# Kernel optimization log

Hardware: AMD Instinct MI355X
Metric: run time of the kernel (lower is better)

Reference implementation:

```python
import jax, jax.numpy as jnp
import numpy as np

B, C, H, W = 4, 64, 256, 256
HEADS = 4
HID = 128  # dim * ffn_expansion_factor
EPS = 1e-5


def _ln_chan(x, w, b):
    # LayerNorm over channel axis of [b,c,h,w] (equiv to to_3d -> LN over c -> to_4d)
    mu = x.mean(1, keepdims=True)
    var = jnp.mean((x - mu) ** 2, axis=1, keepdims=True)
    return (x - mu) / jnp.sqrt(var + EPS) * w[None, :, None, None] + b[None, :, None, None]


def _ln_last(x, w, b):
    mu = x.mean(-1, keepdims=True)
    var = jnp.mean((x - mu) ** 2, axis=-1, keepdims=True)
    return (x - mu) / jnp.sqrt(var + EPS) * w + b


def _conv1(x, Wt):
    # 1x1 conv, no bias; Wt: [out,in]
    return jnp.einsum('oi,bihw->bohw', Wt, x)


def _l2norm(x):
    # torch F.normalize(dim=-1): x / max(||x||, 1e-12)
    return x / jnp.maximum(jnp.linalg.norm(x, axis=-1, keepdims=True), 1e-12)


def _dct(inp1, inp2, Wq, Wk, Wv, temp):
    # Divide_Cross_Transformer: q from inp2, k/v from inp1; channel-wise attention
    b, c, h, w = inp1.shape
    ch = c // HEADS
    hw = h * w
    q = _conv1(inp2, Wq).reshape(b, HEADS, ch, hw)
    k = _conv1(inp1, Wk).reshape(b, HEADS, ch, hw)
    v = _conv1(inp1, Wv).reshape(b, HEADS, ch, hw)
    q = _l2norm(q)
    k = _l2norm(k)
    attn = jax.nn.softmax(jnp.einsum('bhcn,bhdn->bhcd', q, k) * temp[None], axis=-1)
    return attn, v  # attn: [b,head,ch,ch], v: [b,head,ch,hw]


def _ffn(x3, w1, b1, w2, b2):
    # torch nn.GELU default = exact erf
    hdn = jax.nn.gelu(jnp.einsum('bnc,hc->bnh', x3, w1) + b1, approximate=False)
    return jnp.einsum('bnh,ch->bnc', hdn, w2) + b2


def setup_inputs() -> dict:
    key = jax.random.key(0)
    ks = jax.random.split(key, 16)
    s = 0.05

    def n(k, shape):
        return jax.random.normal(k, shape, jnp.float32) * s

    ones = jnp.ones((C,), jnp.float32)
    zeros = jnp.zeros((C,), jnp.float32)
    return {
        'image': jax.random.normal(ks[0], (B, C, H, W), jnp.float32),
        'event': jax.random.normal(ks[1], (B, C, H, W), jnp.float32),
        'Wq_c': n(ks[2], (C, C)), 'Wk_c': n(ks[3], (C, C)), 'Wv_c': n(ks[4], (C, C)),
        'temp_c': jnp.ones((HEADS, 1, 1), jnp.float32),
        'Wq_d': n(ks[5], (C, C)), 'Wk_d': n(ks[6], (C, C)), 'Wv_d': n(ks[7], (C, C)),
        'temp_d': jnp.ones((HEADS, 1, 1), jnp.float32),
        'ln_img_w': ones, 'ln_img_b': zeros,
        'ln_evt_w': ones, 'ln_evt_b': zeros,
        'ln_com_w': ones, 'ln_com_b': zeros,
        'ln_dif_w': ones, 'ln_dif_b': zeros,
        'ln1_w': ones, 'ln1_b': zeros,
        'ln2_w': ones, 'ln2_b': zeros,
        'fc1c_w': n(ks[8], (HID, C)), 'fc1c_b': jnp.zeros((HID,), jnp.float32),
        'fc2c_w': n(ks[9], (C, HID)), 'fc2c_b': jnp.zeros((C,), jnp.float32),
        'fc1d_w': n(ks[10], (HID, C)), 'fc1d_b': jnp.zeros((HID,), jnp.float32),
        'fc2d_w': n(ks[11], (C, HID)), 'fc2d_b': jnp.zeros((C,), jnp.float32),
        'proj1_w': n(ks[12], (C, C)), 'proj2_w': n(ks[13], (C, C)),
    }


def reference(image, event, Wq_c, Wk_c, Wv_c, temp_c, Wq_d, Wk_d, Wv_d, temp_d,
              ln_img_w, ln_img_b, ln_evt_w, ln_evt_b, ln_com_w, ln_com_b,
              ln_dif_w, ln_dif_b, ln1_w, ln1_b, ln2_w, ln2_b,
              fc1c_w, fc1c_b, fc2c_w, fc2c_b, fc1d_w, fc1d_b, fc2d_w, fc2d_b,
              proj1_w, proj2_w):
    b, c, h, w = image.shape
    hw = h * w
    common = image + event
    differential = image - event

    ni = _ln_chan(image, ln_img_w, ln_img_b)
    ne = _ln_chan(event, ln_evt_w, ln_evt_b)
    nc = _ln_chan(common, ln_com_w, ln_com_b)
    nd = _ln_chan(differential, ln_dif_w, ln_dif_b)

    # common branch: shared conv weights (attn_common), attn maps multiplied
    a_ic, v_ic = _dct(ni, nc, Wq_c, Wk_c, Wv_c, temp_c)
    a_ec, v_ec = _dct(ne, nc, Wq_c, Wk_c, Wv_c, temp_c)
    a_c = a_ic * a_ec
    oc = jnp.einsum('bhcd,bhdn->bhcn', a_c, v_ic + v_ec)  # same attn for both matmuls
    oc = oc.reshape(b, c, h, w)
    oc = _conv1(oc, proj1_w)
    oc3 = oc.reshape(b, c, hw).transpose(0, 2, 1)  # b (hw) c
    oc3 = oc3 + _ffn(_ln_last(oc3, ln1_w, ln1_b), fc1c_w, fc1c_b, fc2c_w, fc2c_b)
    out_common = oc3.transpose(0, 2, 1).reshape(b, c, h, w)

    # differential branch: separate attn maps, not multiplied
    a_id, v_id = _dct(ni, nd, Wq_d, Wk_d, Wv_d, temp_d)
    a_ed, v_ed = _dct(ne, nd, Wq_d, Wk_d, Wv_d, temp_d)
    od = (jnp.einsum('bhcd,bhdn->bhcn', a_id, v_id)
          + jnp.einsum('bhcd,bhdn->bhcn', a_ed, v_ed))
    od = od.reshape(b, c, h, w)
    od = _conv1(od, proj2_w)
    od3 = od.reshape(b, c, hw).transpose(0, 2, 1)
    od3 = od3 + _ffn(_ln_last(od3, ln2_w, ln2_b), fc1d_w, fc1d_b, fc2d_w, fc2d_b)
    out_differential = od3.transpose(0, 2, 1).reshape(b, c, h, w)

    return (out_common, out_differential)
```

## Files before the change

### kernel.cpp

```cpp
#include <hip/hip_runtime.h>
#include <math.h>

typedef unsigned int u32;
typedef unsigned short u16;
typedef __attribute__((ext_vector_type(8))) short short8;
typedef __attribute__((ext_vector_type(4))) float float4v;

#define NBATCH 4
#define HW 65536

#define OFF_COV 0
#define OFF_T   131072
#define OFF_M   294912
#define OFF_P   344064
#define OFF_WC  393216
#define OFF_PAR 516096
#define WS_NEED ((size_t)(OFF_PAR + 1048576) * 4)

__device__ inline float bf2f(u16 h){ return __uint_as_float(((u32)h) << 16); }
__device__ inline u16 f2bf(float x){
  u32 u = __float_as_uint(x);
  u += 0x7fffu + ((u >> 16) & 1u);
  return (u16)(u >> 16);
}
__device__ inline u32 packbf2(float a, float b){
  u32 r;
  asm("v_cvt_pk_bf16_f32 %0, %1, %2" : "=v"(r) : "v"(a), "v"(b));
  return r;
}
__device__ inline float bfu(u32 u, int hi){
  return __uint_as_float(hi ? (u & 0xffff0000u) : (u << 16));
}

__device__ inline bool detect_f32(const void* probe, int t, int* s_cnt){
  if (t == 0) *s_cnt = 0;
  __syncthreads();
  u32 w = ((const u32*)probe)[t & 255];
  u32 ex = (w >> 7) & 0xffu;
  if (!(ex >= 113u && ex <= 133u)) atomicAdd(s_cnt, 1);
  __syncthreads();
  return *s_cnt >= 128;
}

__device__ inline bool detect_f32_512(const void* probe, int t, int* s_cnt){
  if (t == 0) *s_cnt = 0;
  __syncthreads();
  if (t < 256){
    u32 w = ((const u32*)probe)[t];
    u32 ex = (w >> 7) & 0xffu;
    if (!(ex >= 113u && ex <= 133u)) atomicAdd(s_cnt, 1);
  }
  __syncthreads();
  return *s_cnt >= 128;
}

__device__ inline void ld8(const u16* pb, const float* pf, size_t idx, bool f32, float* o){
  if (f32){
    const float4 a = *(const float4*)(pf + idx);
    const float4 b = *(const float4*)(pf + idx + 4);
    o[0]=a.x; o[1]=a.y; o[2]=a.z; o[3]=a.w; o[4]=b.x; o[5]=b.y; o[6]=b.z; o[7]=b.w;
  } else {
    uint4 r = *(const uint4*)(pb + idx);
    const u32* p = (const u32*)&r;
    #pragma unroll
    for (int j=0;j<8;j++) o[j] = bfu(p[j>>1], j&1);
  }
}

__device__ inline void ld8_issue(const u16* pb, const float* pf, size_t idx, bool f32, uint4* r2){
  if (f32){
    r2[0] = *(const uint4*)(pf + idx);
    r2[1] = *(const uint4*)(pf + idx + 4);
  } else {
    r2[0] = *(const uint4*)(pb + idx);
  }
}
__device__ inline void ld8_unpack(const uint4* r2, bool f32, float* o){
  if (f32){
    const float* q = (const float*)r2;
    #pragma unroll
    for (int j=0;j<8;j++) o[j] = q[j];
  } else {
    const u32* p = (const u32*)r2;
    #pragma unroll
    for (int j=0;j<8;j++) o[j] = bfu(p[j>>1], j&1);
  }
}

__device__ inline void softmax16(float* l){
  float m = l[0];
  #pragma unroll
  for (int i=1;i<16;i++) m = fmaxf(m, l[i]);
  float s = 0.f;
  #pragma unroll
  for (int i=0;i<16;i++){ l[i] = __expf(l[i]-m); s += l[i]; }
  float r = 1.0f/s;
  #pragma unroll
  for (int i=0;i<16;i++) l[i] *= r;
}

__global__ __launch_bounds__(256) void convert_all(
    const void* img,
    const void* t0, const void* t1, const void* t2, const void* t3,
    const void* t4, const void* t5, const void* t6, const void* t7,
    const void* t8, const void* t9, const void* t10, const void* t11,
    const void* t12, const void* t13, const void* t14, const void* t15,
    const void* t16, const void* t17, const void* t18, const void* t19,
    const void* t20, const void* t21, const void* t22, const void* t23,
    const void* t24, const void* t25, const void* t26, const void* t27,
    const void* t28, const void* t29,
    u16* __restrict__ wc)
{
  __shared__ int s_cnt;
  const int t = threadIdx.x;
  const bool f32 = detect_f32(img, t, &s_cnt);
  const int sizes[30] = {4096,4096,4096,4,4096,4096,4096,4,
                         64,64,64,64,64,64,64,64,64,64,64,64,
                         8192,128,8192,64,8192,128,8192,64,4096,4096};
  const void* srcs[30] = {t0,t1,t2,t3,t4,t5,t6,t7,t8,t9,t10,t11,t12,t13,t14,
                          t15,t16,t17,t18,t19,t20,t21,t22,t23,t24,t25,t26,t27,t28,t29};
  const int id = blockIdx.x;
  const void* s = srcs[id];
  const int n = sizes[id];
  u16* d = wc + (size_t)id*8192;
  for (int j = t; j < n; j += 256)
    d[j] = f32 ? f2bf(((const float*)s)[j]) : ((const u16*)s)[j];
}

__global__ __launch_bounds__(512, 4) void k1_cov(
    const void* __restrict__ img, const void* __restrict__ evt,
    const u16* __restrict__ lniw, const u16* __restrict__ lnib,
    const u16* __restrict__ lnew, const u16* __restrict__ lneb,
    const u16* __restrict__ lncw, const u16* __restrict__ lncb,
    const u16* __restrict__ lndw, const u16* __restrict__ lndb,
    float* __restrict__ cov, float* __restrict__ par, int use_par)
{
  __shared__ u16 NtL[4*64*72];
  __shared__ float spart[8][64][5];
  __shared__ float params[8][64];
  __shared__ int s_cnt;

  const int t = threadIdx.x;
  const bool f32 = detect_f32_512(img, t, &s_cnt);
  const u16* imgb = (const u16*)img; const float* imgf = (const float*)img;
  const u16* evtb = (const u16*)evt; const float* evtf = (const float*)evt;

  const int b = blockIdx.x >> 7;
  const int P0 = (blockIdx.x & 127) * 512;
  const int ch = t >> 3, pg = t & 7;
  const int wave = t >> 6, lane = t & 63, l15 = lane & 15, quad = lane >> 4;

  float wi=bf2f(lniw[ch]), bi=bf2f(lnib[ch]);
  float we=bf2f(lnew[ch]), be=bf2f(lneb[ch]);
  float wc_=bf2f(lncw[ch]), bc_=bf2f(lncb[ch]);
  float wd_=bf2f(lndw[ch]), bd_=bf2f(lndb[ch]);

  const int va = (wave==3)?0 : (wave==7)?1 : (wave<3)?2:3;
  const int vb = (wave==0)?2 : (wave==4)?3 :
                 ((wave==2)||(wave==6)||(wave==7))?1:0;

  float4v acc[4][4];
  #pragma unroll
  for (int i=0;i<4;i++)
    #pragma unroll
    for (int j=0;j<4;j++) acc[i][j]=(float4v)0.f;

  const size_t base = (size_t)(b*64 + ch) * HW;

  for (int it = 0; it < 8; ++it){
    const int p0 = P0 + it*64;
    float A[8], B[8];
    ld8(imgb, imgf, base + p0 + pg*8, f32, A);
    ld8(evtb, evtf, base + p0 + pg*8, f32, B);

    #pragma unroll 1
    for (int jp=0;jp<4;jp++){
      float xa=A[2*jp], xb=A[2*jp+1], ea=B[2*jp], eb=B[2*jp+1];
      float s0a=xa,     s0b=xb;
      float s1a=xa*xa,  s1b=xb*xb;
      float s2a=ea,     s2b=eb;
      float s3a=ea*ea,  s3b=eb*eb;
      float s4a=xa*ea,  s4b=xb*eb;
      #pragma unroll
      for (int m=8;m<=32;m<<=1){
        s0a+=__shfl_xor(s0a,m); s0b+=__shfl_xor(s0b,m);
        s1a+=__shfl_xor(s1a,m); s1b+=__shfl_xor(s1b,m);
        s2a+=__shfl_xor(s2a,m); s2b+=__shfl_xor(s2b,m);
        s3a+=__shfl_xor(s3a,m); s3b+=__shfl_xor(s3b,m);
        s4a+=__shfl_xor(s4a,m); s4b+=__shfl_xor(s4b,m);
      }
      if ((ch&7)==0){
        int px = pg*8 + 2*jp;
        spart[wave][px][0]=s0a; spart[wave][px][1]=s1a; spart[wave][px][2]=s2a;
        spart[wave][px][3]=s3a; spart[wave][px][4]=s4a;
        spart[wave][px+1][0]=s0b; spart[wave][px+1][1]=s1b; spart[wave][px+1][2]=s2b;
        spart[wave][px+1][3]=s3b; spart[wave][px+1][4]=s4b;
      }
    }
    __syncthreads();
    if (t < 64){
      float S0=0,S1=0,S2=0,S3=0,S4=0;
      #pragma unroll
      for (int w=0;w<8;w++){
        S0+=spart[w][t][0]; S1+=spart[w][t][1]; S2+=spart[w][t][2];
        S3+=spart[w][t][3]; S4+=spart[w][t][4];
      }
      const float inv = 0.015625f;
      float mu_i=S0*inv, mu_e=S2*inv;
      float r_i = rsqrtf(fmaf(S1,inv,-mu_i*mu_i)+1e-5f);
      float r_e = rsqrtf(fmaf(S3,inv,-mu_e*mu_e)+1e-5f);
      float mu_c=mu_i+mu_e, mu_d=mu_i-mu_e;
      float r_c = rsqrtf((S1+2.f*S4+S3)*inv - mu_c*mu_c + 1e-5f);
      float r_d = rsqrtf((S1-2.f*S4+S3)*inv - mu_d*mu_d + 1e-5f);
      params[0][t]=mu_i; params[1][t]=r_i; params[2][t]=mu_e; params[3][t]=r_e;
      params[4][t]=mu_c; params[5][t]=r_c; params[6][t]=mu_d; params[7][t]=r_d;
      if (use_par){
        float4 pv; pv.x=mu_i; pv.y=r_i; pv.z=mu_e; pv.w=r_e;
        *(float4*)(par + ((size_t)b*HW + p0 + t)*4) = pv;
      }
    }
    __syncthreads();

    {
      u32 u0[4], u1[4];
      #pragma unroll
      for (int jj=0;jj<4;jj++){
        int px = pg*8 + 2*jj;
        float2 mi01 = *(const float2*)&params[0][px];
        float2 ri01 = *(const float2*)&params[1][px];
        float2 me01 = *(const float2*)&params[2][px];
        float2 re01 = *(const float2*)&params[3][px];
        u0[jj] = packbf2(fmaf((A[2*jj]-mi01.x)*ri01.x, wi, bi),
                         fmaf((A[2*jj+1]-mi01.y)*ri01.y, wi, bi));
        u1[jj] = packbf2(fmaf((B[2*jj]-me01.x)*re01.x, we, be),
                         fmaf((B[2*jj+1]-me01.y)*re01.y, we, be));
      }
      *(uint4*)&NtL[(0*64+ch)*72 + pg*8] = make_uint4(u0[0],u0[1],u0[2],u0[3]);
      *(uint4*)&NtL[(1*64+ch)*72 + pg*8] = make_uint4(u1[0],u1[1],u1[2],u1[3]);
      #pragma unroll
      for (int jj=0;jj<4;jj++){
        int px = pg*8 + 2*jj;
        float2 mc01 = *(const float2*)&params[4][px];
        float2 rc01 = *(const float2*)&params[5][px];
        float2 md01 = *(const float2*)&params[6][px];
        float2 rd01 = *(const float2*)&params[7][px];
        float xc0=A[2*jj]+B[2*jj], xc1=A[2*jj+1]+B[2*jj+1];
        float xd0=A[2*jj]-B[2*jj], xd1=A[2*jj+1]-B[2*jj+1];
        u0[jj] = packbf2(fmaf((xc0-mc01.x)*rc01.x, wc_, bc_),
                         fmaf((xc1-mc01.y)*rc01.y, wc_, bc_));
        u1[jj] = packbf2(fmaf((xd0-md01.x)*rd01.x, wd_, bd_),
                         fmaf((xd1-md01.y)*rd01.y, wd_, bd_));
      }
      *(uint4*)&NtL[(2*64+ch)*72 + pg*8] = make_uint4(u0[0],u0[1],u0[2],u0[3]);
      *(uint4*)&NtL[(3*64+ch)*72 + pg*8] = make_uint4(u1[0],u1[1],u1[2],u1[3]);
    }
    __syncthreads();

    #pragma unroll
    for (int ks=0; ks<2; ks++){
      const int off = ks*32 + quad*8;
      short8 Af[4], Bf[4];
      #pragma unroll
      for (int mi=0;mi<4;mi++){
        Af[mi] = *(const short8*)&NtL[(va*64 + mi*16 + l15)*72 + off];
        Bf[mi] = *(const short8*)&NtL[(vb*64 + mi*16 + l15)*72 + off];
      }
      #pragma unroll
      for (int mi=0;mi<4;mi++)
        #pragma unroll
        for (int nj=0;nj<4;nj++)
          acc[mi][nj] = __builtin_amdgcn_mfma_f32_16x16x32_bf16(Af[mi], Bf[nj], acc[mi][nj], 0,0,0);
    }
  }
  float* cg = cov + ((size_t)wave*NBATCH + b)*4096;
  #pragma unroll
  for (int mi=0;mi<4;mi++)
    #pragma unroll
    for (int nj=0;nj<4;nj++){
      int row0 = mi*16 + quad*4, col = nj*16 + l15;
      #pragma unroll
      for (int r=0;r<4;r++)
        atomicAdd(&cg[(row0+r)*64 + col], acc[mi][nj][r]);
    }
}

__global__ __launch_bounds__(256) void p2a(
    const u16* __restrict__ Wq_c, const u16* __restrict__ Wk_c,
    const u16* __restrict__ Wq_d, const u16* __restrict__ Wk_d,
    float* __restrict__ ws)
{
  __shared__ float WL[64][65];
  __shared__ float CL[64][64];
  const int t = threadIdx.x;
  const int b = blockIdx.x & 3;
  const int which = blockIdx.x >> 2;
  int wsel, csel;
  switch (which){
    case 0: wsel=0; csel=0; break;
    case 1: wsel=1; csel=3; break;
    case 2: wsel=1; csel=7; break;
    case 3: wsel=2; csel=4; break;
    case 4: wsel=3; csel=3; break;
    case 5: wsel=3; csel=7; break;
    case 6: wsel=0; csel=1; break;
    case 7: wsel=0; csel=2; break;
    case 8: wsel=2; csel=5; break;
    default: wsel=2; csel=6; break;
  }
  const u16* W = (wsel==0)? Wq_c : (wsel==1)? Wk_c : (wsel==2)? Wq_d : Wk_d;
  const float* Cm = ws + ((size_t)csel*NBATCH + b)*4096;
  { int r = t>>2, c0 = (t&3)*16;
    #pragma unroll
    for (int i=0;i<16;i++) WL[r][c0+i] = bf2f(W[r*64 + c0 + i]);
    const float4* s = (const float4*)(Cm + r*64 + c0);
    float4* d = (float4*)&CL[r][c0];
    d[0]=s[0]; d[1]=s[1]; d[2]=s[2]; d[3]=s[3]; }
  __syncthreads();
  const int r = t>>2, k0 = (t&3)*16;
  float a[16];
  #pragma unroll
  for (int i=0;i<16;i++) a[i]=0.f;
  for (int m=0;m<64;m++){
    float wv = WL[r][m];
    #pragma unroll
    for (int i=0;i<16;i++) a[i] = fmaf(wv, CL[m][k0+i], a[i]);
  }
  float* o = ws + OFF_T + ((size_t)which*NBATCH + b)*4096 + r*64 + k0;
  #pragma unroll
  for (int i=0;i<16;i++) o[i] = a[i];
}

__global__ __launch_bounds__(256) void p2b(
    float* __restrict__ ws,
    const u16* __restrict__ Wq_c, const u16* __restrict__ Wk_c,
    const u16* __restrict__ Wq_d, const u16* __restrict__ Wk_d,
    const u16* __restrict__ Wv_c, const u16* __restrict__ Wv_d,
    const u16* __restrict__ temp_c, const u16* __restrict__ temp_d)
{
  const int b = blockIdx.x, t = threadIdx.x;
  __shared__ float rn[6][64];
  __shared__ float GLs[4][64][16];
  __shared__ float AL[3][64][16];
  const float* T = ws + OFF_T;
  {
    int s = t>>6, c = t&63;
    const float* Tp = T + ((size_t)s*NBATCH + b)*4096 + c*64;
    const u16* Wp = (s==0)? Wq_c : (s==3)? Wq_d : Wk_c;
    float acc=0;
    for (int k=0;k<64;k++) acc = fmaf(Tp[k], bf2f(Wp[c*64+k]), acc);
    rn[s][c] = 1.0f/fmaxf(sqrtf(fmaxf(acc,0.f)), 1e-12f);
    if (t < 128){
      int s2 = 4 + (t>>6);
      const float* Tp2 = T + ((size_t)s2*NBATCH + b)*4096 + c*64;
      float acc2=0;
      for (int k=0;k<64;k++) acc2 = fmaf(Tp2[k], bf2f(Wk_d[c*64+k]), acc2);
      rn[s2][c] = 1.0f/fmaxf(sqrtf(fmaxf(acc2,0.f)), 1e-12f);
    }
  }
  #pragma unroll 1
  for (int i=0;i<16;i++){
    int e = t*16 + i;
    int s = e >> 10, c = (e>>4)&63, dl = e&15, d = (c&~15)+dl;
    const float* Tp = T + ((size_t)(6+s)*NBATCH + b)*4096 + c*64;
    const u16* Wp = ((s<2)? Wk_c : Wk_d) + d*64;
    float acc=0;
    for (int j=0;j<64;j++) acc = fmaf(Tp[j], bf2f(Wp[j]), acc);
    GLs[s][c][dl] = acc;
  }
  __syncthreads();
  if (t < 192){
    int set = t>>6, c = t&63, h = c>>4, cb = c&~15;
    if (set == 0){
      float tc = bf2f(temp_c[h]);
      float rq = rn[0][c];
      float l1[16], l2[16];
      #pragma unroll
      for (int dl=0;dl<16;dl++){
        l1[dl] = GLs[0][c][dl]*rq*rn[1][cb+dl]*tc;
        l2[dl] = GLs[1][c][dl]*rq*rn[2][cb+dl]*tc;
      }
      softmax16(l1); softmax16(l2);
      #pragma unroll
      for (int dl=0;dl<16;dl++) AL[0][c][dl] = l1[dl]*l2[dl];
    } else {
      float td = bf2f(temp_d[h]);
      float rq = rn[3][c];
      int gi = (set==1)? 2 : 3;
      int rk = (set==1)? 4 : 5;
      float l[16];
      #pragma unroll
      for (int dl=0;dl<16;dl++) l[dl] = GLs[gi][c][dl]*rq*rn[rk][cb+dl]*td;
      softmax16(l);
      #pragma unroll
      for (int dl=0;dl<16;dl++) AL[set][c][dl] = l[dl];
    }
  }
  __syncthreads();
  for (int wsel=0; wsel<3; wsel++){
    const u16* Wv = (wsel==0)? Wv_c : Wv_d;
    #pragma unroll 1
    for (int i=0;i<16;i++){
      int e = t*16+i, c = e>>6, k = e&63, cb = c&~15;
      float acc=0;
      #pragma unroll
      for (int dl=0;dl<16;dl++) acc = fmaf(AL[wsel][c][dl], bf2f(Wv[(cb+dl)*64 + k]), acc);
      ws[OFF_M + ((size_t)wsel*NBATCH + b)*4096 + c*64 + k] = acc;
    }
  }
}

__global__ __launch_bounds__(256) void p2c(
    const u16* __restrict__ proj1, const u16* __restrict__ proj2,
    float* __restrict__ ws)
{
  __shared__ float WL[64][65];
  __shared__ float CL[64][64];
  const int t = threadIdx.x;
  const int b = blockIdx.x & 3;
  const int which = blockIdx.x >> 2;
  const u16* W = (which==0)? proj1 : proj2;
  const float* Cm = ws + OFF_M + ((size_t)which*NBATCH + b)*4096;
  { int r = t>>2, c0 = (t&3)*16;
    #pragma unroll
    for (int i=0;i<16;i++) WL[r][c0+i] = bf2f(W[r*64 + c0 + i]);
    const float4* s = (const float4*)(Cm + r*64 + c0);
    float4* d = (float4*)&CL[r][c0];
    d[0]=s[0]; d[1]=s[1]; d[2]=s[2]; d[3]=s[3]; }
  __syncthreads();
  const int r = t>>2, k0 = (t&3)*16;
  float a[16];
  #pragma unroll
  for (int i=0;i<16;i++) a[i]=0.f;
  for (int m=0;m<64;m++){
    float wv = WL[r][m];
    #pragma unroll
    for (int i=0;i<16;i++) a[i] = fmaf(wv, CL[m][k0+i], a[i]);
  }
  float* o = ws + OFF_P + ((size_t)which*NBATCH + b)*4096 + r*64 + k0;
  #pragma unroll
  for (int i=0;i<16;i++) o[i] = a[i];
}

__global__ __launch_bounds__(256, 2) void k3_common(
    const void* __restrict__ img, const void* __restrict__ evt,
    const u16* __restrict__ lniw, const u16* __restrict__ lnib,
    const u16* __restrict__ lnew, const u16* __restrict__ lneb,
    const u16* __restrict__ ln1w, const u16* __restrict__ ln1b,
    const u16* __restrict__ fc1w, const u16* __restrict__ fc1b,
    const u16* __restrict__ fc2w, const u16* __restrict__ fc2b,
    const float* __restrict__ Pmat, void* __restrict__ outp, size_t obase,
    const float* __restrict__ par, int use_par)
{
  __shared__ u16 fc1L[128*72];
  __shared__ u16 fc2L[64*136];
  __shared__ u16 PcL[64*72];
  __shared__ u16 SB[64*136];
  __shared__ float spart[4][64][4];
  __shared__ float params[64][4];
  __shared__ float b1L[128];
  __shared__ float b2L[64];
  __shared__ int s_cnt;

  const int t = threadIdx.x;
  const bool f32 = detect_f32(img, t, &s_cnt);
  const u16* imgb = (const u16*)img; const float* imgf = (const float*)img;
  const u16* evtb = (const u16*)evt; const float* evtf = (const float*)evt;

  const int b = blockIdx.x >> 8;
  const int P0 = (blockIdx.x & 255) * 256;
  const int chg = t >> 3, pg = t & 7, ch0 = chg*2;
  const int wave = t >> 6, lane = t & 63, l15 = lane & 15, quad = lane >> 4;

  { int row = t >> 1, c0 = (t & 1)*32;
    const uint4* s = (const uint4*)(fc1w + row*64 + c0);
    uint4* d = (uint4*)&fc1L[row*72 + c0];
    d[0]=s[0]; d[1]=s[1]; d[2]=s[2]; d[3]=s[3]; }
  { int row = t >> 2, c0 = (t & 3)*32;
    const uint4* s = (const uint4*)(fc2w + row*128 + c0);
    uint4* d = (uint4*)&fc2L[row*136 + c0];
    d[0]=s[0]; d[1]=s[1]; d[2]=s[2]; d[3]=s[3]; }
  { int row = t >> 2, c0 = (t & 3)*16;
    const float* s = Pmat + (size_t)b*4096 + row*64 + c0;
    u32 u[8];
    #pragma unroll
    for (int i=0;i<8;i++) u[i] = packbf2(s[2*i], s[2*i+1]);
    uint4* d = (uint4*)&PcL[row*72 + c0];
    d[0] = make_uint4(u[0],u[1],u[2],u[3]);
    d[1] = make_uint4(u[4],u[5],u[6],u[7]); }
  if (t < 128) b1L[t] = bf2f(fc1b[t]);
  if (t < 64)  b2L[t] = bf2f(fc2b[t]);

  float wi0=bf2f(lniw[ch0]), wi1=bf2f(lniw[ch0+1]);
  float we0=bf2f(lnew[ch0]), we1=bf2f(lnew[ch0+1]);
  float bs0=bf2f(lnib[ch0]) + bf2f(lneb[ch0]);
  float bs1=bf2f(lnib[ch0+1]) + bf2f(lneb[ch0+1]);
  float w1r[4], b1r[4];
  #pragma unroll
  for (int nj=0;nj<4;nj++){ w1r[nj]=bf2f(ln1w[nj*16+l15]); b1r[nj]=bf2f(ln1b[nj*16+l15]); }

  const size_t base_i = (size_t)(b*64 + ch0)*HW;
  uint4 rA0[2], rA1[2], rB0[2], rB1[2];
  float4 PR[8];
  if (use_par){
    ld8_issue(imgb, imgf, base_i + P0 + pg*8, f32, rA0);
    ld8_issue(imgb, imgf, base_i + HW + P0 + pg*8, f32, rA1);
    ld8_issue(evtb, evtf, base_i + P0 + pg*8, f32, rB0);
    ld8_issue(evtb, evtf, base_i + HW + P0 + pg*8, f32, rB1);
    const float4* pp = (const float4*)(par + ((size_t)b*HW + P0 + pg*8)*4);
    #pragma unroll
    for (int j=0;j<8;j++) PR[j] = pp[j];
  }
  __syncthreads();

  for (int it=0; it<4; ++it){
    const int p0 = P0 + it*64;
    if (use_par){
      float A0[8], A1[8], B0[8], B1[8];
      ld8_unpack(rA0, f32, A0); ld8_unpack(rA1, f32, A1);
      ld8_unpack(rB0, f32, B0); ld8_unpack(rB1, f32, B1);
      #pragma unroll
      for (int j=0;j<8;j++){
        float4 pr = PR[j];
        float a0=(A0[j]-pr.x)*pr.y, a1=(A1[j]-pr.x)*pr.y;
        float c0f=(B0[j]-pr.z)*pr.w, c1f=(B1[j]-pr.z)*pr.w;
        float n0 = fmaf(a0, wi0, fmaf(c0f, we0, bs0));
        float n1 = fmaf(a1, wi1, fmaf(c1f, we1, bs1));
        *(u32*)&SB[(pg*8+j)*136 + ch0] = packbf2(n0, n1);
      }
    } else {
      float A0[8], A1[8], B0[8], B1[8];
      ld8(imgb, imgf, base_i + p0 + pg*8, f32, A0);
      ld8(imgb, imgf, base_i + HW + p0 + pg*8, f32, A1);
      ld8(evtb, evtf, base_i + p0 + pg*8, f32, B0);
      ld8(evtb, evtf, base_i + HW + p0 + pg*8, f32, B1);
      float si[8], sii[8], se[8], see[8];
      #pragma unroll
      for (int j=0;j<8;j++){
        float xi0=A0[j], xi1=A1[j], xe0=B0[j], xe1=B1[j];
        si[j]=xi0+xi1; sii[j]=fmaf(xi0,xi0,xi1*xi1);
        se[j]=xe0+xe1; see[j]=fmaf(xe0,xe0,xe1*xe1);
      }
      #pragma unroll
      for (int m=8;m<=32;m<<=1)
        #pragma unroll
        for (int j=0;j<8;j++){
          si[j]+=__shfl_xor(si[j],m); sii[j]+=__shfl_xor(sii[j],m);
          se[j]+=__shfl_xor(se[j],m); see[j]+=__shfl_xor(see[j],m);
        }
      if ((chg&7)==0){
        #pragma unroll
        for (int j=0;j<8;j++){
          spart[wave][pg*8+j][0]=si[j]; spart[wave][pg*8+j][1]=sii[j];
          spart[wave][pg*8+j][2]=se[j]; spart[wave][pg*8+j][3]=see[j];
        }
      }
      __syncthreads();
      if (t<64){
        float S0=0,S1=0,S2=0,S3=0;
        #pragma unroll
        for (int w=0;w<4;w++){ S0+=spart[w][t][0]; S1+=spart[w][t][1]; S2+=spart[w][t][2]; S3+=spart[w][t][3]; }
        const float inv=0.015625f;
        float mu_i=S0*inv, mu_e=S2*inv;
        float r_i=rsqrtf(fmaf(S1,inv,-mu_i*mu_i)+1e-5f);
        float r_e=rsqrtf(fmaf(S3,inv,-mu_e*mu_e)+1e-5f);
        params[t][0]=mu_i; params[t][1]=r_i; params[t][2]=mu_e; params[t][3]=r_e;
      }
      __syncthreads();
      #pragma unroll
      for (int j=0;j<8;j++){
        float4 pr = *(const float4*)&params[pg*8+j][0];
        float a0=(A0[j]-pr.x)*pr.y, a1=(A1[j]-pr.x)*pr.y;
        float c0f=(B0[j]-pr.z)*pr.w, c1f=(B1[j]-pr.z)*pr.w;
        float n0 = fmaf(a0, wi0, fmaf(c0f, we0, bs0));
        float n1 = fmaf(a1, wi1, fmaf(c1f, we1, bs1));
        *(u32*)&SB[(pg*8+j)*136 + ch0] = packbf2(n0, n1);
      }
    }
    __syncthreads();
    if (use_par && it < 3){
      const int pn = p0 + 64;
      ld8_issue(imgb, imgf, base_i + pn + pg*8, f32, rA0);
      ld8_issue(imgb, imgf, base_i + HW + pn + pg*8, f32, rA1);
      ld8_issue(evtb, evtf, base_i + pn + pg*8, f32, rB0);
      ld8_issue(evtb, evtf, base_i + HW + pn + pg*8, f32, rB1);
      const float4* pp = (const float4*)(par + ((size_t)b*HW + pn + pg*8)*4);
      #pragma unroll
      for (int j=0;j<8;j++) PR[j] = pp[j];
    }
    float4v acc1[4];
    #pragma unroll
    for (int nj=0;nj<4;nj++) acc1[nj]=(float4v)0.f;
    const int px_row = wave*16 + l15;
    #pragma unroll
    for (int ks=0;ks<2;ks++){
      const int off = ks*32 + quad*8;
      short8 af = *(const short8*)&SB[px_row*136 + off];
      #pragma unroll
      for (int nj=0;nj<4;nj++){
        short8 bw = *(const short8*)&PcL[(nj*16+l15)*72 + off];
        acc1[nj] = __builtin_amdgcn_mfma_f32_16x16x32_bf16(af, bw, acc1[nj], 0,0,0);
      }
    }
    float s[4], sq[4];
    #pragma unroll
    for (int j=0;j<4;j++){
      s[j] = acc1[0][j]+acc1[1][j]+acc1[2][j]+acc1[3][j];
      sq[j] = acc1[0][j]*acc1[0][j];
      sq[j] = fmaf(acc1[1][j],acc1[1][j],sq[j]);
      sq[j] = fmaf(acc1[2][j],acc1[2][j],sq[j]);
      sq[j] = fmaf(acc1[3][j],acc1[3][j],sq[j]);
    }
    #pragma unroll
    for (int m=1;m<=8;m<<=1)
      #pragma unroll
      for (int j=0;j<4;j++){ s[j]+=__shfl_xor(s[j],m); sq[j]+=__shfl_xor(sq[j],m); }
    float muj[4], rj[4];
    #pragma unroll
    for (int j=0;j<4;j++){
      muj[j]=s[j]*0.015625f;
      rj[j]=rsqrtf(fmaf(sq[j],0.015625f,-muj[j]*muj[j])+1e-5f);
    }
    #pragma unroll
    for (int nj=0;nj<4;nj++)
      #pragma unroll
      for (int j=0;j<4;j++){
        float tv = (acc1[nj][j]-muj[j])*rj[j];
        tv = fmaf(tv, w1r[nj], b1r[nj]);
        SB[(wave*16+quad*4+j)*136 + nj*16+l15] = f2bf(tv);
      }
    float4v accF[8];
    #pragma unroll
    for (int nh=0;nh<8;nh++) accF[nh]=(float4v)0.f;
    #pragma unroll
    for (int ks=0;ks<2;ks++){
      const int off = ks*32+quad*8;
      short8 af = *(const short8*)&SB[px_row*136 + off];
      #pragma unroll
      for (int nh=0;nh<8;nh++){
        short8 bw = *(const short8*)&fc1L[(nh*16+l15)*72 + off];
        accF[nh] = __builtin_amdgcn_mfma_f32_16x16x32_bf16(af, bw, accF[nh], 0,0,0);
      }
    }
    #pragma unroll
    for (int nh=0;nh<8;nh++){
      float bb = b1L[nh*16+l15];
      #pragma unroll
      for (int j=0;j<4;j++){
        float v = accF[nh][j] + bb;
        float g = 0.5f*v*(1.0f + erff(v*0.70710678118654752f));
        SB[(wave*16+quad*4+j)*136 + nh*16+l15] = f2bf(g);
      }
    }
    float4v accO[4];
    #pragma unroll
    for (int nj=0;nj<4;nj++) accO[nj]=(float4v)0.f;
    #pragma unroll
    for (int ks=0;ks<4;ks++){
      const int off = ks*32+quad*8;
      short8 ag = *(const short8*)&SB[px_row*136 + off];
      #pragma unroll
      for (int nj=0;nj<4;nj++){
        short8 bw = *(const short8*)&fc2L[(nj*16+l15)*136 + off];
        accO[nj] = __builtin_amdgcn_mfma_f32_16x16x32_bf16(ag, bw, accO[nj], 0,0,0);
      }
    }
    const int px0 = p0 + wave*16 + quad*4;
    #pragma unroll
    for (int nj=0;nj<4;nj++){
      float bb = b2L[nj*16+l15];
      int r = nj*16+l15;
      float v0 = acc1[nj][0] + accO[nj][0] + bb;
      float v1 = acc1[nj][1] + accO[nj][1] + bb;
      float v2 = acc1[nj][2] + accO[nj][2] + bb;
      float v3 = acc1[nj][3] + accO[nj][3] + bb;
      size_t oi = obase + (size_t)(b*64 + r)*HW + px0;
      if (f32){ float4 fv; fv.x=v0; fv.y=v1; fv.z=v2; fv.w=v3;
        *(float4*)((float*)outp + oi) = fv; }
      else *(uint2*)((u16*)outp + oi) = make_uint2(packbf2(v0,v1), packbf2(v2,v3));
    }
    __syncthreads();
  }
}

__global__ __launch_bounds__(256, 2) void k3_diff(
    const void* __restrict__ img, const void* __restrict__ evt,
    const u16* __restrict__ lniw, const u16* __restrict__ lnib,
    const u16* __restrict__ lnew, const u16* __restrict__ lneb,
    const u16* __restrict__ ln2w, const u16* __restrict__ ln2b,
    const u16* __restrict__ fc1w, const u16* __restrict__ fc1b,
    const u16* __restrict__ fc2w, const u16* __restrict__ fc2b,
    const float* __restrict__ Pmat, void* __restrict__ outp, size_t obase,
    const float* __restrict__ par, int use_par)
{
  __shared__ u16 fc1L[128*72];
  __shared__ u16 fc2L[64*136];
  __shared__ u16 PiL[64*72];
  __shared__ u16 PeL[64*72];
  __shared__ u16 N2L[64*144];
  __shared__ float spart[4][64][4];
  __shared__ float params[64][4];
  __shared__ float b1L[128];
  __shared__ float b2L[64];
  __shared__ int s_cnt;

  const int t = threadIdx.x;
  const bool f32 = detect_f32(img, t, &s_cnt);
  const u16* imgb = (const u16*)img; const float* imgf = (const float*)img;
  const u16* evtb = (const u16*)evt; const float* evtf = (const float*)evt;

  const int b = blockIdx.x >> 8;
  const int P0 = (blockIdx.x & 255) * 256;
  const int chg = t >> 3, pg = t & 7, ch0 = chg*2;
  const int wave = t >> 6, lane = t & 63, l15 = lane & 15, quad = lane >> 4;

  { int row = t >> 1, c0 = (t & 1)*32;
    const uint4* s = (const uint4*)(fc1w + row*64 + c0);
    uint4* d = (uint4*)&fc1L[row*72 + c0];
    d[0]=s[0]; d[1]=s[1]; d[2]=s[2]; d[3]=s[3]; }
  { int row = t >> 2, c0 = (t & 3)*32;
    const uint4* s = (const uint4*)(fc2w + row*128 + c0);
    uint4* d = (uint4*)&fc2L[row*136 + c0];
    d[0]=s[0]; d[1]=s[1]; d[2]=s[2]; d[3]=s[3]; }
  { int row = t >> 2, c0 = (t & 3)*16;
    const float* si_ = Pmat + ((size_t)1*NBATCH + b)*4096 + row*64 + c0;
    const float* se_ = Pmat + ((size_t)2*NBATCH + b)*4096 + row*64 + c0;
    u32 u[8];
    #pragma unroll
    for (int i=0;i<8;i++) u[i] = packbf2(si_[2*i], si_[2*i+1]);
    uint4* d = (uint4*)&PiL[row*72 + c0];
    d[0] = make_uint4(u[0],u[1],u[2],u[3]); d[1] = make_uint4(u[4],u[5],u[6],u[7]);
    #pragma unroll
    for (int i=0;i<8;i++) u[i] = packbf2(se_[2*i], se_[2*i+1]);
    uint4* d2 = (uint4*)&PeL[row*72 + c0];
    d2[0] = make_uint4(u[0],u[1],u[2],u[3]); d2[1] = make_uint4(u[4],u[5],u[6],u[7]); }
  if (t < 128) b1L[t] = bf2f(fc1b[t]);
  if (t < 64)  b2L[t] = bf2f(fc2b[t]);

  float wi0=bf2f(lniw[ch0]), wi1=bf2f(lniw[ch0+1]);
  float bi0=bf2f(lnib[ch0]), bi1=bf2f(lnib[ch0+1]);
  float we0=bf2f(lnew[ch0]), we1=bf2f(lnew[ch0+1]);
  float be0=bf2f(lneb[ch0]), be1=bf2f(lneb[ch0+1]);
  float w1r[4], b1r[4];
  #pragma unroll
  for (int nj=0;nj<4;nj++){ w1r[nj]=bf2f(ln2w[nj*16+l15]); b1r[nj]=bf2f(ln2b[nj*16+l15]); }

  const size_t base_i = (size_t)(b*64 + ch0)*HW;
  uint4 rA0[2], rA1[2], rB0[2], rB1[2];
  float4 PR[8];
  if (use_par){
    ld8_issue(imgb, imgf, base_i + P0 + pg*8, f32, rA0);
    ld8_issue(imgb, imgf, base_i + HW + P0 + pg*8, f32, rA1);
    ld8_issue(evtb, evtf, base_i + P0 + pg*8, f32, rB0);
    ld8_issue(evtb, evtf, base_i + HW + P0 + pg*8, f32, rB1);
    const float4* pp = (const float4*)(par + ((size_t)b*HW + P0 + pg*8)*4);
    #pragma unroll
    for (int j=0;j<8;j++) PR[j] = pp[j];
  }
  __syncthreads();

  for (int it=0; it<4; ++it){
    const int p0 = P0 + it*64;
    if (use_par){
      float A0[8], A1[8], B0[8], B1[8];
      ld8_unpack(rA0, f32, A0); ld8_unpack(rA1, f32, A1);
      ld8_unpack(rB0, f32, B0); ld8_unpack(rB1, f32, B1);
      #pragma unroll
      for (int j=0;j<8;j++){
        float4 pr = PR[j];
        float a0=(A0[j]-pr.x)*pr.y, a1=(A1[j]-pr.x)*pr.y;
        float c0f=(B0[j]-pr.z)*pr.w, c1f=(B1[j]-pr.z)*pr.w;
        *(u32*)&N2L[(pg*8+j)*144 + ch0]      = packbf2(fmaf(a0,wi0,bi0), fmaf(a1,wi1,bi1));
        *(u32*)&N2L[(pg*8+j)*144 + 72 + ch0] = packbf2(fmaf(c0f,we0,be0), fmaf(c1f,we1,be1));
      }
    } else {
      float A0[8], A1[8], B0[8], B1[8];
      ld8(imgb, imgf, base_i + p0 + pg*8, f32, A0);
      ld8(imgb, imgf, base_i + HW + p0 + pg*8, f32, A1);
      ld8(evtb, evtf, base_i + p0 + pg*8, f32, B0);
      ld8(evtb, evtf, base_i + HW + p0 + pg*8, f32, B1);
      float si[8], sii[8], se[8], see[8];
      #pragma unroll
      for (int j=0;j<8;j++){
        float xi0=A0[j], xi1=A1[j], xe0=B0[j], xe1=B1[j];
        si[j]=xi0+xi1; sii[j]=fmaf(xi0,xi0,xi1*xi1);
        se[j]=xe0+xe1; see[j]=fmaf(xe0,xe0,xe1*xe1);
      }
      #pragma unroll
      for (int m=8;m<=32;m<<=1)
        #pragma unroll
        for (int j=0;j<8;j++){
          si[j]+=__shfl_xor(si[j],m); sii[j]+=__shfl_xor(sii[j],m);
          se[j]+=__shfl_xor(se[j],m); see[j]+=__shfl_xor(see[j],m);
        }
      if ((chg&7)==0){
        #pragma unroll
        for (int j=0;j<8;j++){
          spart[wave][pg*8+j][0]=si[j]; spart[wave][pg*8+j][1]=sii[j];
          spart[wave][pg*8+j][2]=se[j]; spart[wave][pg*8+j][3]=see[j];
        }
      }
      __syncthreads();
      if (t<64){
        float S0=0,S1=0,S2=0,S3=0;
        #pragma unroll
        for (int w=0;w<4;w++){ S0+=spart[w][t][0]; S1+=spart[w][t][1]; S2+=spart[w][t][2]; S3+=spart[w][t][3]; }
        const float inv=0.015625f;
        float mu_i=S0*inv, mu_e=S2*inv;
        float r_i=rsqrtf(fmaf(S1,inv,-mu_i*mu_i)+1e-5f);
        float r_e=rsqrtf(fmaf(S3,inv,-mu_e*mu_e)+1e-5f);
        params[t][0]=mu_i; params[t][1]=r_i; params[t][2]=mu_e; params[t][3]=r_e;
      }
      __syncthreads();
      #pragma unroll
      for (int j=0;j<8;j++){
        float4 pr = *(const float4*)&params[pg*8+j][0];
        float a0=(A0[j]-pr.x)*pr.y, a1=(A1[j]-pr.x)*pr.y;
        float c0f=(B0[j]-pr.z)*pr.w, c1f=(B1[j]-pr.z)*pr.w;
        *(u32*)&N2L[(pg*8+j)*144 + ch0]      = packbf2(fmaf(a0,wi0,bi0), fmaf(a1,wi1,bi1));
        *(u32*)&N2L[(pg*8+j)*144 + 72 + ch0] = packbf2(fmaf(c0f,we0,be0), fmaf(c1f,we1,be1));
      }
    }
    __syncthreads();
    if (use_par && it < 3){
      const int pn = p0 + 64;
      ld8_issue(imgb, imgf, base_i + pn + pg*8, f32, rA0);
      ld8_issue(imgb, imgf, base_i + HW + pn + pg*8, f32, rA1);
      ld8_issue(evtb, evtf, base_i + pn + pg*8, f32, rB0);
      ld8_issue(evtb, evtf, base_i + HW + pn + pg*8, f32, rB1);
      const float4* pp = (const float4*)(par + ((size_t)b*HW + pn + pg*8)*4);
      #pragma unroll
      for (int j=0;j<8;j++) PR[j] = pp[j];
    }
    float4v acc1[4];
    #pragma unroll
    for (int nj=0;nj<4;nj++) acc1[nj]=(float4v)0.f;
    const int px_row = wave*16 + l15;
    #pragma unroll
    for (int ks=0;ks<2;ks++){
      const int off = ks*32 + quad*8;
      short8 ai = *(const short8*)&N2L[px_row*144 + off];
      short8 ae = *(const short8*)&N2L[px_row*144 + 72 + off];
      #pragma unroll
      for (int nj=0;nj<4;nj++){
        short8 bwi = *(const short8*)&PiL[(nj*16+l15)*72 + off];
        acc1[nj] = __builtin_amdgcn_mfma_f32_16x16x32_bf16(ai, bwi, acc1[nj], 0,0,0);
        short8 bwe = *(const short8*)&PeL[(nj*16+l15)*72 + off];
        acc1[nj] = __builtin_amdgcn_mfma_f32_16x16x32_bf16(ae, bwe, acc1[nj], 0,0,0);
      }
    }
    float s[4], sq[4];
    #pragma unroll
    for (int j=0;j<4;j++){
      s[j] = acc1[0][j]+acc1[1][j]+acc1[2][j]+acc1[3][j];
      sq[j] = acc1[0][j]*acc1[0][j];
      sq[j] = fmaf(acc1[1][j],acc1[1][j],sq[j]);
      sq[j] = fmaf(acc1[2][j],acc1[2][j],sq[j]);
      sq[j] = fmaf(acc1[3][j],acc1[3][j],sq[j]);
    }
    #pragma unroll
    for (int m=1;m<=8;m<<=1)
      #pragma unroll
      for (int j=0;j<4;j++){ s[j]+=__shfl_xor(s[j],m); sq[j]+=__shfl_xor(sq[j],m); }
    float muj[4], rj[4];
    #pragma unroll
    for (int j=0;j<4;j++){
      muj[j]=s[j]*0.015625f;
      rj[j]=rsqrtf(fmaf(sq[j],0.015625f,-muj[j]*muj[j])+1e-5f);
    }
    #pragma unroll
    for (int nj=0;nj<4;nj++)
      #pragma unroll
      for (int j=0;j<4;j++){
        float tv = (acc1[nj][j]-muj[j])*rj[j];
        tv = fmaf(tv, w1r[nj], b1r[nj]);
        N2L[(wave*16+quad*4+j)*144 + nj*16+l15] = f2bf(tv);
      }
    float4v accF[8];
    #pragma unroll
    for (int nh=0;nh<8;nh++) accF[nh]=(float4v)0.f;
    #pragma unroll
    for (int ks=0;ks<2;ks++){
      const int off = ks*32+quad*8;
      short8 af = *(const short8*)&N2L[px_row*144 + off];
      #pragma unroll
      for (int nh=0;nh<8;nh++){
        short8 bw = *(const short8*)&fc1L[(nh*16+l15)*72 + off];
        accF[nh] = __builtin_amdgcn_mfma_f32_16x16x32_bf16(af, bw, accF[nh], 0,0,0);
      }
    }
    #pragma unroll
    for (int nh=0;nh<8;nh++){
      float bb = b1L[nh*16+l15];
      #pragma unroll
      for (int j=0;j<4;j++){
        float v = accF[nh][j] + bb;
        float g = 0.5f*v*(1.0f + erff(v*0.70710678118654752f));
        N2L[(wave*16+quad*4+j)*144 + nh*16+l15] = f2bf(g);
      }
    }
    float4v accO[4];
    #pragma unroll
    for (int nj=0;nj<4;nj++) accO[nj]=(float4v)0.f;
    #pragma unroll
    for (int ks=0;ks<4;ks++){
      const int off = ks*32+quad*8;
      short8 ag = *(const short8*)&N2L[px_row*144 + off];
      #pragma unroll
      for (int nj=0;nj<4;nj++){
        short8 bw = *(const short8*)&fc2L[(nj*16+l15)*136 + off];
        accO[nj] = __builtin_amdgcn_mfma_f32_16x16x32_bf16(ag, bw, accO[nj], 0,0,0);
      }
    }
    const int px0 = p0 + wave*16 + quad*4;
    #pragma unroll
    for (int nj=0;nj<4;nj++){
      float bb = b2L[nj*16+l15];
      int r = nj*16+l15;
      float v0 = acc1[nj][0] + accO[nj][0] + bb;
      float v1 = acc1[nj][1] + accO[nj][1] + bb;
      float v2 = acc1[nj][2] + accO[nj][2] + bb;
      float v3 = acc1[nj][3] + accO[nj][3] + bb;
      size_t oi = obase + (size_t)(b*64 + r)*HW + px0;
      if (f32){ float4 fv; fv.x=v0; fv.y=v1; fv.z=v2; fv.w=v3;
        *(float4*)((float*)outp + oi) = fv; }
      else *(uint2*)((u16*)outp + oi) = make_uint2(packbf2(v0,v1), packbf2(v2,v3));
    }
    __syncthreads();
  }
}

extern "C" void kernel_launch(void* const* d_in, const int* in_sizes, int n_in,
                              void* d_out, int out_size, void* d_ws, size_t ws_size,
                              hipStream_t stream)
{
  const void* img = d_in[0];
  const void* evt = d_in[1];
  float* ws = (float*)d_ws;
  u16* wc = (u16*)(ws + OFF_WC);
  float* par = ws + OFF_PAR;
  const int use_par = (ws_size >= WS_NEED) ? 1 : 0;
  #define SLOT(i) (wc + (size_t)((i)-2)*8192)

  hipMemsetAsync(ws, 0, 131072*sizeof(float), stream);
  convert_all<<<dim3(30), dim3(256), 0, stream>>>(img,
      d_in[2], d_in[3], d_in[4], d_in[5], d_in[6], d_in[7], d_in[8], d_in[9],
      d_in[10], d_in[11], d_in[12], d_in[13], d_in[14], d_in[15], d_in[16], d_in[17],
      d_in[18], d_in[19], d_in[20], d_in[21], d_in[22], d_in[23], d_in[24], d_in[25],
      d_in[26], d_in[27], d_in[28], d_in[29], d_in[30], d_in[31], wc);
  k1_cov<<<dim3(512), dim3(512), 0, stream>>>(img, evt,
      SLOT(10), SLOT(11), SLOT(12), SLOT(13), SLOT(14), SLOT(15), SLOT(16), SLOT(17),
      ws, par, use_par);
  p2a<<<dim3(40), dim3(256), 0, stream>>>(SLOT(2), SLOT(3), SLOT(6), SLOT(7), ws);
  p2b<<<dim3(4), dim3(256), 0, stream>>>(ws, SLOT(2), SLOT(3), SLOT(6), SLOT(7),
      SLOT(4), SLOT(8), SLOT(5), SLOT(9));
  p2c<<<dim3(12), dim3(256), 0, stream>>>(SLOT(30), SLOT(31), ws);
  k3_common<<<dim3(1024), dim3(256), 0, stream>>>(img, evt,
      SLOT(10), SLOT(11), SLOT(12), SLOT(13), SLOT(18), SLOT(19),
      SLOT(22), SLOT(23), SLOT(24), SLOT(25), ws + OFF_P, d_out, (size_t)0, par, use_par);
  k3_diff<<<dim3(1024), dim3(256), 0, stream>>>(img, evt,
      SLOT(10), SLOT(11), SLOT(12), SLOT(13), SLOT(20), SLOT(21),
      SLOT(26), SLOT(27), SLOT(28), SLOT(29), ws + OFF_P, d_out, (size_t)16777216, par, use_par);
  #undef SLOT
}
```

Measured before the change: 562.0 us.

## Fuse small attention-prep kernels and merge common/diff output kernels into one launch

Folds the workspace memset into extra convert_all blocks, and fuses p2a/p2b/p2c into one 4-block kernel that loops over the small matmuls serially. k3_common and k3_diff become a single k3_fat launch with interleaved blocks that pick their branch by block parity. The aim is to remove launch overhead and the tail gaps between kernels, and to let both branches share image/event reads in L2. The cost is that the fused p2 stage has far less parallelism (4 blocks doing serial loops), and branch selection adds a little divergence and register pressure inside k3_fat.

Measured after the change: 605.7 us. +7.8%, slower.

```diff
diff --git a/kernel.cpp b/kernel.cpp
--- a/kernel.cpp
+++ b/kernel.cpp
@@ -42,7 +42,7 @@
   return *s_cnt >= 128;
 }
 
-__device__ inline bool detect_f32_512(const void* probe, int t, int* s_cnt){
+__device__ inline bool detect_f32_wide(const void* probe, int t, int* s_cnt){
   if (t == 0) *s_cnt = 0;
   __syncthreads();
   if (t < 256){
@@ -109,17 +109,23 @@
     const void* t20, const void* t21, const void* t22, const void* t23,
     const void* t24, const void* t25, const void* t26, const void* t27,
     const void* t28, const void* t29,
-    u16* __restrict__ wc)
+    u16* __restrict__ wc, float* __restrict__ cov)
 {
   __shared__ int s_cnt;
   const int t = threadIdx.x;
   const bool f32 = detect_f32(img, t, &s_cnt);
+  const int id = blockIdx.x;
+  if (id >= 30){
+    float4 z; z.x=0.f; z.y=0.f; z.z=0.f; z.w=0.f;
+    float4* c4 = (float4*)cov + (size_t)(id-30)*16384;
+    for (int j = t; j < 16384; j += 256) c4[j] = z;
+    return;
+  }
   const int sizes[30] = {4096,4096,4096,4,4096,4096,4096,4,
                          64,64,64,64,64,64,64,64,64,64,64,64,
                          8192,128,8192,64,8192,128,8192,64,4096,4096};
   const void* srcs[30] = {t0,t1,t2,t3,t4,t5,t6,t7,t8,t9,t10,t11,t12,t13,t14,
                           t15,t16,t17,t18,t19,t20,t21,t22,t23,t24,t25,t26,t27,t28,t29};
-  const int id = blockIdx.x;
   const void* s = srcs[id];
   const int n = sizes[id];
   u16* d = wc + (size_t)id*8192;
@@ -141,7 +147,7 @@
   __shared__ int s_cnt;
 
   const int t = threadIdx.x;
-  const bool f32 = detect_f32_512(img, t, &s_cnt);
+  const bool f32 = detect_f32_wide(img, t, &s_cnt);
   const u16* imgb = (const u16*)img; const float* imgf = (const float*)img;
   const u16* evtb = (const u16*)evt; const float* evtf = (const float*)evt;
 
@@ -284,63 +290,52 @@
     }
 }
 
-__global__ __launch_bounds__(256) void p2a(
+__global__ __launch_bounds__(256) void p2_fused(
     const u16* __restrict__ Wq_c, const u16* __restrict__ Wk_c,
     const u16* __restrict__ Wq_d, const u16* __restrict__ Wk_d,
+    const u16* __restrict__ Wv_c, const u16* __restrict__ Wv_d,
+    const u16* __restrict__ temp_c, const u16* __restrict__ temp_d,
+    const u16* __restrict__ proj1, const u16* __restrict__ proj2,
     float* __restrict__ ws)
 {
   __shared__ float WL[64][65];
   __shared__ float CL[64][64];
-  const int t = threadIdx.x;
-  const int b = blockIdx.x & 3;
-  const int which = blockIdx.x >> 2;
-  int wsel, csel;
-  switch (which){
-    case 0: wsel=0; csel=0; break;
-    case 1: wsel=1; csel=3; break;
-    case 2: wsel=1; csel=7; break;
-    case 3: wsel=2; csel=4; break;
-    case 4: wsel=3; csel=3; break;
-    case 5: wsel=3; csel=7; break;
-    case 6: wsel=0; csel=1; break;
-    case 7: wsel=0; csel=2; break;
-    case 8: wsel=2; csel=5; break;
-    default: wsel=2; csel=6; break;
-  }
-  const u16* W = (wsel==0)? Wq_c : (wsel==1)? Wk_c : (wsel==2)? Wq_d : Wk_d;
-  const float* Cm = ws + ((size_t)csel*NBATCH + b)*4096;
-  { int r = t>>2, c0 = (t&3)*16;
-    #pragma unroll
-    for (int i=0;i<16;i++) WL[r][c0+i] = bf2f(W[r*64 + c0 + i]);
-    const float4* s = (const float4*)(Cm + r*64 + c0);
-    float4* d = (float4*)&CL[r][c0];
-    d[0]=s[0]; d[1]=s[1]; d[2]=s[2]; d[3]=s[3]; }
-  __syncthreads();
-  const int r = t>>2, k0 = (t&3)*16;
-  float a[16];
-  #pragma unroll
-  for (int i=0;i<16;i++) a[i]=0.f;
-  for (int m=0;m<64;m++){
-    float wv = WL[r][m];
-    #pragma unroll
-    for (int i=0;i<16;i++) a[i] = fmaf(wv, CL[m][k0+i], a[i]);
-  }
-  float* o = ws + OFF_T + ((size_t)which*NBATCH + b)*4096 + r*64 + k0;
-  #pragma unroll
-  for (int i=0;i<16;i++) o[i] = a[i];
-}
-
-__global__ __launch_bounds__(256) void p2b(
-    float* __restrict__ ws,
-    const u16* __restrict__ Wq_c, const u16* __restrict__ Wk_c,
-    const u16* __restrict__ Wq_d, const u16* __restrict__ Wk_d,
-    const u16* __restrict__ Wv_c, const u16* __restrict__ Wv_d,
-    const u16* __restrict__ temp_c, const u16* __restrict__ temp_d)
-{
-  const int b = blockIdx.x, t = threadIdx.x;
   __shared__ float rn[6][64];
   __shared__ float GLs[4][64][16];
   __shared__ float AL[3][64][16];
+  const int t = threadIdx.x;
+  const int b = blockIdx.x;
+
+  const int wsel_tab[10] = {0,1,1,2,3,3,0,0,2,2};
+  const int csel_tab[10] = {0,3,7,4,3,7,1,2,5,6};
+  #pragma unroll 1
+  for (int which=0; which<10; ++which){
+    const int wsel = wsel_tab[which], csel = csel_tab[which];
+    const u16* W = (wsel==0)? Wq_c : (wsel==1)? Wk_c : (wsel==2)? Wq_d : Wk_d;
+    const float* Cm = ws + ((size_t)csel*NBATCH + b)*4096;
+    __syncthreads();
+    { int r = t>>2, c0 = (t&3)*16;
+      #pragma unroll
+      for (int i=0;i<16;i++) WL[r][c0+i] = bf2f(W[r*64 + c0 + i]);
+      const float4* s = (const float4*)(Cm + r*64 + c0);
+      float4* d = (float4*)&CL[r][c0];
+      d[0]=s[0]; d[1]=s[1]; d[2]=s[2]; d[3]=s[3]; }
+    __syncthreads();
+    const int r = t>>2, k0 = (t&3)*16;
+    float a[16];
+    #pragma unroll
+    for (int i=0;i<16;i++) a[i]=0.f;
+    for (int m=0;m<64;m++){
+      float wv = WL[r][m];
+      #pragma unroll
+      for (int i=0;i<16;i++) a[i] = fmaf(wv, CL[m][k0+i], a[i]);
+    }
+    float* o = ws + OFF_T + ((size_t)which*NBATCH + b)*4096 + r*64 + k0;
+    #pragma unroll
+    for (int i=0;i<16;i++) o[i] = a[i];
+  }
+  __syncthreads();
+
   const float* T = ws + OFF_T;
   {
     int s = t>>6, c = t&63;
@@ -407,69 +402,80 @@
       ws[OFF_M + ((size_t)wsel*NBATCH + b)*4096 + c*64 + k] = acc;
     }
   }
-}
-
-__global__ __launch_bounds__(256) void p2c(
-    const u16* __restrict__ proj1, const u16* __restrict__ proj2,
-    float* __restrict__ ws)
-{
-  __shared__ float WL[64][65];
-  __shared__ float CL[64][64];
-  const int t = threadIdx.x;
-  const int b = blockIdx.x & 3;
-  const int which = blockIdx.x >> 2;
-  const u16* W = (which==0)? proj1 : proj2;
-  const float* Cm = ws + OFF_M + ((size_t)which*NBATCH + b)*4096;
-  { int r = t>>2, c0 = (t&3)*16;
-    #pragma unroll
-    for (int i=0;i<16;i++) WL[r][c0+i] = bf2f(W[r*64 + c0 + i]);
-    const float4* s = (const float4*)(Cm + r*64 + c0);
-    float4* d = (float4*)&CL[r][c0];
-    d[0]=s[0]; d[1]=s[1]; d[2]=s[2]; d[3]=s[3]; }
-  __syncthreads();
-  const int r = t>>2, k0 = (t&3)*16;
-  float a[16];
-  #pragma unroll
-  for (int i=0;i<16;i++) a[i]=0.f;
-  for (int m=0;m<64;m++){
-    float wv = WL[r][m];
-    #pragma unroll
-    for (int i=0;i<16;i++) a[i] = fmaf(wv, CL[m][k0+i], a[i]);
-  }
-  float* o = ws + OFF_P + ((size_t)which*NBATCH + b)*4096 + r*64 + k0;
-  #pragma unroll
-  for (int i=0;i<16;i++) o[i] = a[i];
-}
-
-__global__ __launch_bounds__(256, 2) void k3_common(
+  __syncthreads();
+
+  #pragma unroll 1
+  for (int which=0; which<3; ++which){
+    const u16* W = (which==0)? proj1 : proj2;
+    const float* Cm = ws + OFF_M + ((size_t)which*NBATCH + b)*4096;
+    __syncthreads();
+    { int r = t>>2, c0 = (t&3)*16;
+      #pragma unroll
+      for (int i=0;i<16;i++) WL[r][c0+i] = bf2f(W[r*64 + c0 + i]);
+      const float4* s = (const float4*)(Cm + r*64 + c0);
+      float4* d = (float4*)&CL[r][c0];
+      d[0]=s[0]; d[1]=s[1]; d[2]=s[2]; d[3]=s[3]; }
+    __syncthreads();
+    const int r = t>>2, k0 = (t&3)*16;
+    float a[16];
+    #pragma unroll
+    for (int i=0;i<16;i++) a[i]=0.f;
+    for (int m=0;m<64;m++){
+      float wv = WL[r][m];
+      #pragma unroll
+      for (int i=0;i<16;i++) a[i] = fmaf(wv, CL[m][k0+i], a[i]);
+    }
+    float* o = ws + OFF_P + ((size_t)which*NBATCH + b)*4096 + r*64 + k0;
+    #pragma unroll
+    for (int i=0;i<16;i++) o[i] = a[i];
+  }
+}
+
+__global__ __launch_bounds__(256, 2) void k3_fat(
     const void* __restrict__ img, const void* __restrict__ evt,
     const u16* __restrict__ lniw, const u16* __restrict__ lnib,
     const u16* __restrict__ lnew, const u16* __restrict__ lneb,
     const u16* __restrict__ ln1w, const u16* __restrict__ ln1b,
-    const u16* __restrict__ fc1w, const u16* __restrict__ fc1b,
-    const u16* __restrict__ fc2w, const u16* __restrict__ fc2b,
-    const float* __restrict__ Pmat, void* __restrict__ outp, size_t obase,
+    const u16* __restrict__ ln2w, const u16* __restrict__ ln2b,
+    const u16* __restrict__ fc1cw, const u16* __restrict__ fc1cb,
+    const u16* __restrict__ fc2cw, const u16* __restrict__ fc2cb,
+    const u16* __restrict__ fc1dw, const u16* __restrict__ fc1db,
+    const u16* __restrict__ fc2dw, const u16* __restrict__ fc2db,
+    const float* __restrict__ Pmat, void* __restrict__ outp,
     const float* __restrict__ par, int use_par)
 {
-  __shared__ u16 fc1L[128*72];
-  __shared__ u16 fc2L[64*136];
-  __shared__ u16 PcL[64*72];
-  __shared__ u16 SB[64*136];
+  __shared__ __align__(16) u16 POOL[36352];
   __shared__ float spart[4][64][4];
   __shared__ float params[64][4];
   __shared__ float b1L[128];
   __shared__ float b2L[64];
   __shared__ int s_cnt;
 
+  u16* fc1L = POOL;
+  u16* fc2L = POOL + 9216;
+  u16* P0L  = POOL + 17920;
+  u16* P1L  = POOL + 22528;
+  u16* BIG  = POOL + 27136;
+
   const int t = threadIdx.x;
   const bool f32 = detect_f32(img, t, &s_cnt);
   const u16* imgb = (const u16*)img; const float* imgf = (const float*)img;
   const u16* evtb = (const u16*)evt; const float* evtf = (const float*)evt;
 
-  const int b = blockIdx.x >> 8;
-  const int P0 = (blockIdx.x & 255) * 256;
+  const int isdiff = blockIdx.x & 1;
+  const int g = blockIdx.x >> 1;
+  const int b = g >> 8;
+  const int P0 = (g & 255) * 256;
+  const size_t obase = isdiff ? (size_t)16777216 : (size_t)0;
   const int chg = t >> 3, pg = t & 7, ch0 = chg*2;
   const int wave = t >> 6, lane = t & 63, l15 = lane & 15, quad = lane >> 4;
+
+  const u16* fc1w = isdiff ? fc1dw : fc1cw;
+  const u16* fc1b = isdiff ? fc1db : fc1cb;
+  const u16* fc2w = isdiff ? fc2dw : fc2cw;
+  const u16* fc2b = isdiff ? fc2db : fc2cb;
+  const u16* lnfw = isdiff ? ln2w : ln1w;
+  const u16* lnfb = isdiff ? ln2b : ln1b;
 
   { int row = t >> 1, c0 = (t & 1)*32;
     const uint4* s = (const uint4*)(fc1w + row*64 + c0);
@@ -479,24 +485,40 @@
     const uint4* s = (const uint4*)(fc2w + row*128 + c0);
     uint4* d = (uint4*)&fc2L[row*136 + c0];
     d[0]=s[0]; d[1]=s[1]; d[2]=s[2]; d[3]=s[3]; }
-  { int row = t >> 2, c0 = (t & 3)*16;
+  if (!isdiff){
+    int row = t >> 2, c0 = (t & 3)*16;
     const float* s = Pmat + (size_t)b*4096 + row*64 + c0;
     u32 u[8];
     #pragma unroll
     for (int i=0;i<8;i++) u[i] = packbf2(s[2*i], s[2*i+1]);
-    uint4* d = (uint4*)&PcL[row*72 + c0];
+    uint4* d = (uint4*)&P0L[row*72 + c0];
     d[0] = make_uint4(u[0],u[1],u[2],u[3]);
-    d[1] = make_uint4(u[4],u[5],u[6],u[7]); }
+    d[1] = make_uint4(u[4],u[5],u[6],u[7]);
+  } else {
+    int row = t >> 2, c0 = (t & 3)*16;
+    const float* si_ = Pmat + ((size_t)1*NBATCH + b)*4096 + row*64 + c0;
+    const float* se_ = Pmat + ((size_t)2*NBATCH + b)*4096 + row*64 + c0;
+    u32 u[8];
+    #pragma unroll
+    for (int i=0;i<8;i++) u[i] = packbf2(si_[2*i], si_[2*i+1]);
+    uint4* d = (uint4*)&P0L[row*72 + c0];
+    d[0] = make_uint4(u[0],u[1],u[2],u[3]); d[1] = make_uint4(u[4],u[5],u[6],u[7]);
+    #pragma unroll
+    for (int i=0;i<8;i++) u[i] = packbf2(se_[2*i], se_[2*i+1]);
+    uint4* d2 = (uint4*)&P1L[row*72 + c0];
+    d2[0] = make_uint4(u[0],u[1],u[2],u[3]); d2[1] = make_uint4(u[4],u[5],u[6],u[7]);
+  }
   if (t < 128) b1L[t] = bf2f(fc1b[t]);
   if (t < 64)  b2L[t] = bf2f(fc2b[t]);
 
   float wi0=bf2f(lniw[ch0]), wi1=bf2f(lniw[ch0+1]);
   float we0=bf2f(lnew[ch0]), we1=bf2f(lnew[ch0+1]);
-  float bs0=bf2f(lnib[ch0]) + bf2f(lneb[ch0]);
-  float bs1=bf2f(lnib[ch0+1]) + bf2f(lneb[ch0+1]);
+  float bi0=bf2f(lnib[ch0]), bi1=bf2f(lnib[ch0+1]);
+  float be0=bf2f(lneb[ch0]), be1=bf2f(lneb[ch0+1]);
+  float bs0=bi0+be0, bs1=bi1+be1;
   float w1r[4], b1r[4];
   #pragma unroll
-  for (int nj=0;nj<4;nj++){ w1r[nj]=bf2f(ln1w[nj*16+l15]); b1r[nj]=bf2f(ln1b[nj*16+l15]); }
+  for (int nj=0;nj<4;nj++){ w1r[nj]=bf2f(lnfw[nj*16+l15]); b1r[nj]=bf2f(lnfb[nj*16+l15]); }
 
   const size_t base_i = (size_t)(b*64 + ch0)*HW;
   uint4 rA0[2], rA1[2], rB0[2], rB1[2];
@@ -512,20 +534,32 @@
   }
   __syncthreads();
 
+  const int STRIDE = isdiff ? 144 : 136;
   for (int it=0; it<4; ++it){
     const int p0 = P0 + it*64;
     if (use_par){
       float A0[8], A1[8], B0[8], B1[8];
       ld8_unpack(rA0, f32, A0); ld8_unpack(rA1, f32, A1);
       ld8_unpack(rB0, f32, B0); ld8_unpack(rB1, f32, B1);
-      #pragma unroll
-      for (int j=0;j<8;j++){
-        float4 pr = PR[j];
-        float a0=(A0[j]-pr.x)*pr.y, a1=(A1[j]-pr.x)*pr.y;
-        float c0f=(B0[j]-pr.z)*pr.w, c1f=(B1[j]-pr.z)*pr.w;
-        float n0 = fmaf(a0, wi0, fmaf(c0f, we0, bs0));
-        float n1 = fmaf(a1, wi1, fmaf(c1f, we1, bs1));
-        *(u32*)&SB[(pg*8+j)*136 + ch0] = packbf2(n0, n1);
+      if (!isdiff){
+        #pragma unroll
+        for (int j=0;j<8;j++){
+          float4 pr = PR[j];
+          float a0=(A0[j]-pr.x)*pr.y, a1=(A1[j]-pr.x)*pr.y;
+          float c0f=(B0[j]-pr.z)*pr.w, c1f=(B1[j]-pr.z)*pr.w;
+          float n0 = fmaf(a0, wi0, fmaf(c0f, we0, bs0));
+          float n1 = fmaf(a1, wi1, fmaf(c1f, we1, bs1));
+          *(u32*)&BIG[(pg*8+j)*136 + ch0] = packbf2(n0, n1);
+        }
+      } else {
+        #pragma unroll
+        for (int j=0;j<8;j++){
+          float4 pr = PR[j];
+          float a0=(A0[j]-pr.x)*pr.y, a1=(A1[j]-pr.x)*pr.y;
+          float c0f=(B0[j]-pr.z)*pr.w, c1f=(B1[j]-pr.z)*pr.w;
+          *(u32*)&BIG[(pg*8+j)*144 + ch0]      = packbf2(fmaf(a0,wi0,bi0), fmaf(a1,wi1,bi1));
+          *(u32*)&BIG[(pg*8+j)*144 + 72 + ch0] = packbf2(fmaf(c0f,we0,be0), fmaf(c1f,we1,be1));
+        }
       }
     } else {
       float A0[8], A1[8], B0[8], B1[8];
@@ -566,14 +600,25 @@
         params[t][0]=mu_i; params[t][1]=r_i; params[t][2]=mu_e; params[t][3]=r_e;
       }
       __syncthreads();
-      #pragma unroll
-      for (int j=0;j<8;j++){
-        float4 pr = *(const float4*)&params[pg*8+j][0];
-        float a0=(A0[j]-pr.x)*pr.y, a1=(A1[j]-pr.x)*pr.y;
-        float c0f=(B0[j]-pr.z)*pr.w, c1f=(B1[j]-pr.z)*pr.w;
-        float n0 = fmaf(a0, wi0, fmaf(c0f, we0, bs0));
-        float n1 = fmaf(a1, wi1, fmaf(c1f, we1, bs1));
-        *(u32*)&SB[(pg*8+j)*136 + ch0] = packbf2(n0, n1);
+      if (!isdiff){
+        #pragma unroll
+        for (int j=0;j<8;j++){
+          float4 pr = *(const float4*)&params[pg*8+j][0];
+          float a0=(A0[j]-pr.x)*pr.y, a1=(A1[j]-pr.x)*pr.y;
+          float c0f=(B0[j]-pr.z)*pr.w, c1f=(B1[j]-pr.z)*pr.w;
+          float n0 = fmaf(a0, wi0, fmaf(c0f, we0, bs0));
+          float n1 = fmaf(a1, wi1, fmaf(c1f, we1, bs1));
+          *(u32*)&BIG[(pg*8+j)*136 + ch0] = packbf2(n0, n1);
+        }
+      } else {
+        #pragma unroll
+        for (int j=0;j<8;j++){
+          float4 pr = *(const float4*)&params[pg*8+j][0];
+          float a0=(A0[j]-pr.x)*pr.y, a1=(A1[j]-pr.x)*pr.y;
+          float c0f=(B0[j]-pr.z)*pr.w, c1f=(B1[j]-pr.z)*pr.w;
+          *(u32*)&BIG[(pg*8+j)*144 + ch0]      = packbf2(fmaf(a0,wi0,bi0), fmaf(a1,wi1,bi1));
+          *(u32*)&BIG[(pg*8+j)*144 + 72 + ch0] = packbf2(fmaf(c0f,we0,be0), fmaf(c1f,we1,be1));
+        }
       }
     }
     __syncthreads();
@@ -591,14 +636,30 @@
     #pragma unroll
     for (int nj=0;nj<4;nj++) acc1[nj]=(float4v)0.f;
     const int px_row = wave*16 + l15;
-    #pragma unroll
-    for (int ks=0;ks<2;ks++){
-      const int off = ks*32 + quad*8;
-      short8 af = *(const short8*)&SB[px_row*136 + off];
-      #pragma unroll
-      for (int nj=0;nj<4;nj++){
-        short8 bw = *(const short8*)&PcL[(nj*16+l15)*72 + off];
-        acc1[nj] = __builtin_amdgcn_mfma_f32_16x16x32_bf16(af, bw, acc1[nj], 0,0,0);
+    if (!isdiff){
+      #pragma unroll
+      for (int ks=0;ks<2;ks++){
+        const int off = ks*32 + quad*8;
+        short8 af = *(const short8*)&BIG[px_row*136 + off];
+        #pragma unroll
+        for (int nj=0;nj<4;nj++){
+          short8 bw = *(const short8*)&P0L[(nj*16+l15)*72 + off];
+          acc1[nj] = __builtin_amdgcn_mfma_f32_16x16x32_bf16(af, bw, acc1[nj], 0,0,0);
+        }
+      }
+    } else {
+      #pragma unroll
+      for (int ks=0;ks<2;ks++){
+        const int off = ks*32 + quad*8;
+        short8 ai = *(const short8*)&BIG[px_row*144 + off];
+        short8 ae = *(const short8*)&BIG[px_row*144 + 72 + off];
+        #pragma unroll
+        for (int nj=0;nj<4;nj++){
+          short8 bwi = *(const short8*)&P0L[(nj*16+l15)*72 + off];
+          acc1[nj] = __builtin_amdgcn_mfma_f32_16x16x32_bf16(ai, bwi, acc1[nj], 0,0,0);
+          short8 bwe = *(const short8*)&P1L[(nj*16+l15)*72 + off];
+          acc1[nj] = __builtin_amdgcn_mfma_f32_16x16x32_bf16(ae, bwe, acc1[nj], 0,0,0);
+        }
       }
     }
     float s[4], sq[4];
@@ -626,7 +687,7 @@
       for (int j=0;j<4;j++){
         float tv = (acc1[nj][j]-muj[j])*rj[j];
         tv = fmaf(tv, w1r[nj], b1r[nj]);
-        SB[(wave*16+quad*4+j)*136 + nj*16+l15] = f2bf(tv);
+        BIG[(wave*16+quad*4+j)*STRIDE + nj*16+l15] = f2bf(tv);
       }
     float4v accF[8];
     #pragma unroll
@@ -634,7 +695,7 @@
     #pragma unroll
     for (int ks=0;ks<2;ks++){
       const int off = ks*32+quad*8;
-      short8 af = *(const short8*)&SB[px_row*136 + off];
+      short8 af = *(const short8*)&BIG[px_row*STRIDE + off];
       #pragma unroll
       for (int nh=0;nh<8;nh++){
         short8 bw = *(const short8*)&fc1L[(nh*16+l15)*72 + off];
@@ -647,8 +708,8 @@
       #pragma unroll
       for (int j=0;j<4;j++){
         float v = accF[nh][j] + bb;
-        float g = 0.5f*v*(1.0f + erff(v*0.70710678118654752f));
-        SB[(wave*16+quad*4+j)*136 + nh*16+l15] = f2bf(g);
+        float g2 = 0.5f*v*(1.0f + erff(v*0.70710678118654752f));
+        BIG[(wave*16+quad*4+j)*STRIDE + nh*16+l15] = f2bf(g2);
       }
     }
     float4v accO[4];
@@ -657,7 +718,7 @@
     #pragma unroll
     for (int ks=0;ks<4;ks++){
       const int off = ks*32+quad*8;
-      short8 ag = *(const short8*)&SB[px_row*136 + off];
+      short8 ag = *(const short8*)&BIG[px_row*STRIDE + off];
       #pragma unroll
       for (int nj=0;nj<4;nj++){
         short8 bw = *(const short8*)&fc2L[(nj*16+l15)*136 + off];
@@ -682,253 +743,6 @@
   }
 }
 
-__global__ __launch_bounds__(256, 2) void k3_diff(
-    const void* __restrict__ img, const void* __restrict__ evt,
-    const u16* __restrict__ lniw, const u16* __restrict__ lnib,
-    const u16* __restrict__ lnew, const u16* __restrict__ lneb,
-    const u16* __restrict__ ln2w, const u16* __restrict__ ln2b,
-    const u16* __restrict__ fc1w, const u16* __restrict__ fc1b,
-    const u16* __restrict__ fc2w, const u16* __restrict__ fc2b,
-    const float* __restrict__ Pmat, void* __restrict__ outp, size_t obase,
-    const float* __restrict__ par, int use_par)
-{
-  __shared__ u16 fc1L[128*72];
-  __shared__ u16 fc2L[64*136];
-  __shared__ u16 PiL[64*72];
-  __shared__ u16 PeL[64*72];
-  __shared__ u16 N2L[64*144];
-  __shared__ float spart[4][64][4];
-  __shared__ float params[64][4];
-  __shared__ float b1L[128];
-  __shared__ float b2L[64];
-  __shared__ int s_cnt;
-
-  const int t = threadIdx.x;
-  const bool f32 = detect_f32(img, t, &s_cnt);
-  const u16* imgb = (const u16*)img; const float* imgf = (const float*)img;
-  const u16* evtb = (const u16*)evt; const float* evtf = (const float*)evt;
-
-  const int b = blockIdx.x >> 8;
-  const int P0 = (blockIdx.x & 255) * 256;
-  const int chg = t >> 3, pg = t & 7, ch0 = chg*2;
-  const int wave = t >> 6, lane = t & 63, l15 = lane & 15, quad = lane >> 4;
-
-  { int row = t >> 1, c0 = (t & 1)*32;
-    const uint4* s = (const uint4*)(fc1w + row*64 + c0);
-    uint4* d = (uint4*)&fc1L[row*72 + c0];
-    d[0]=s[0]; d[1]=s[1]; d[2]=s[2]; d[3]=s[3]; }
-  { int row = t >> 2, c0 = (t & 3)*32;
-    const uint4* s = (const uint4*)(fc2w + row*128 + c0);
-    uint4* d = (uint4*)&fc2L[row*136 + c0];
-    d[0]=s[0]; d[1]=s[1]; d[2]=s[2]; d[3]=s[3]; }
-  { int row = t >> 2, c0 = (t & 3)*16;
-    const float* si_ = Pmat + ((size_t)1*NBATCH + b)*4096 + row*64 + c0;
-    const float* se_ = Pmat + ((size_t)2*NBATCH + b)*4096 + row*64 + c0;
-    u32 u[8];
-    #pragma unroll
-    for (int i=0;i<8;i++) u[i] = packbf2(si_[2*i], si_[2*i+1]);
-    uint4* d = (uint4*)&PiL[row*72 + c0];
-    d[0] = make_uint4(u[0],u[1],u[2],u[3]); d[1] = make_uint4(u[4],u[5],u[6],u[7]);
-    #pragma unroll
-    for (int i=0;i<8;i++) u[i] = packbf2(se_[2*i], se_[2*i+1]);
-    uint4* d2 = (uint4*)&PeL[row*72 + c0];
-    d2[0] = make_uint4(u[0],u[1],u[2],u[3]); d2[1] = make_uint4(u[4],u[5],u[6],u[7]); }
-  if (t < 128) b1L[t] = bf2f(fc1b[t]);
-  if (t < 64)  b2L[t] = bf2f(fc2b[t]);
-
-  float wi0=bf2f(lniw[ch0]), wi1=bf2f(lniw[ch0+1]);
-  float bi0=bf2f(lnib[ch0]), bi1=bf2f(lnib[ch0+1]);
-  float we0=bf2f(lnew[ch0]), we1=bf2f(lnew[ch0+1]);
-  float be0=bf2f(lneb[ch0]), be1=bf2f(lneb[ch0+1]);
-  float w1r[4], b1r[4];
-  #pragma unroll
-  for (int nj=0;nj<4;nj++){ w1r[nj]=bf2f(ln2w[nj*16+l15]); b1r[nj]=bf2f(ln2b[nj*16+l15]); }
-
-  const size_t base_i = (size_t)(b*64 + ch0)*HW;
-  uint4 rA0[2], rA1[2], rB0[2], rB1[2];
-  float4 PR[8];
-  if (use_par){
-    ld8_issue(imgb, imgf, base_i + P0 + pg*8, f32, rA0);
-    ld8_issue(imgb, imgf, base_i + HW + P0 + pg*8, f32, rA1);
-    ld8_issue(evtb, evtf, base_i + P0 + pg*8, f32, rB0);
-    ld8_issue(evtb, evtf, base_i + HW + P0 + pg*8, f32, rB1);
-    const float4* pp = (const float4*)(par + ((size_t)b*HW + P0 + pg*8)*4);
-    #pragma unroll
-    for (int j=0;j<8;j++) PR[j] = pp[j];
-  }
-  __syncthreads();
-
-  for (int it=0; it<4; ++it){
-    const int p0 = P0 + it*64;
-    if (use_par){
-      float A0[8], A1[8], B0[8], B1[8];
-      ld8_unpack(rA0, f32, A0); ld8_unpack(rA1, f32, A1);
-      ld8_unpack(rB0, f32, B0); ld8_unpack(rB1, f32, B1);
-      #pragma unroll
-      for (int j=0;j<8;j++){
-        float4 pr = PR[j];
-        float a0=(A0[j]-pr.x)*pr.y, a1=(A1[j]-pr.x)*pr.y;
-        float c0f=(B0[j]-pr.z)*pr.w, c1f=(B1[j]-pr.z)*pr.w;
-        *(u32*)&N2L[(pg*8+j)*144 + ch0]      = packbf2(fmaf(a0,wi0,bi0), fmaf(a1,wi1,bi1));
-        *(u32*)&N2L[(pg*8+j)*144 + 72 + ch0] = packbf2(fmaf(c0f,we0,be0), fmaf(c1f,we1,be1));
-      }
-    } else {
-      float A0[8], A1[8], B0[8], B1[8];
-      ld8(imgb, imgf, base_i + p0 + pg*8, f32, A0);
-      ld8(imgb, imgf, base_i + HW + p0 + pg*8, f32, A1);
-      ld8(evtb, evtf, base_i + p0 + pg*8, f32, B0);
-      ld8(evtb, evtf, base_i + HW + p0 + pg*8, f32, B1);
-      float si[8], sii[8], se[8], see[8];
-      #pragma unroll
-      for (int j=0;j<8;j++){
-        float xi0=A0[j], xi1=A1[j], xe0=B0[j], xe1=B1[j];
-        si[j]=xi0+xi1; sii[j]=fmaf(xi0,xi0,xi1*xi1);
-        se[j]=xe0+xe1; see[j]=fmaf(xe0,xe0,xe1*xe1);
-      }
-      #pragma unroll
-      for (int m=8;m<=32;m<<=1)
-        #pragma unroll
-        for (int j=0;j<8;j++){
-          si[j]+=__shfl_xor(si[j],m); sii[j]+=__shfl_xor(sii[j],m);
-          se[j]+=__shfl_xor(se[j],m); see[j]+=__shfl_xor(see[j],m);
-        }
-      if ((chg&7)==0){
-        #pragma unroll
-        for (int j=0;j<8;j++){
-          spart[wave][pg*8+j][0]=si[j]; spart[wave][pg*8+j][1]=sii[j];
-          spart[wave][pg*8+j][2]=se[j]; spart[wave][pg*8+j][3]=see[j];
-        }
-      }
-      __syncthreads();
-      if (t<64){
-        float S0=0,S1=0,S2=0,S3=0;
-        #pragma unroll
-        for (int w=0;w<4;w++){ S0+=spart[w][t][0]; S1+=spart[w][t][1]; S2+=spart[w][t][2]; S3+=spart[w][t][3]; }
-        const float inv=0.015625f;
-        float mu_i=S0*inv, mu_e=S2*inv;
-        float r_i=rsqrtf(fmaf(S1,inv,-mu_i*mu_i)+1e-5f);
-        float r_e=rsqrtf(fmaf(S3,inv,-mu_e*mu_e)+1e-5f);
-        params[t][0]=mu_i; params[t][1]=r_i; params[t][2]=mu_e; params[t][3]=r_e;
-      }
-      __syncthreads();
-      #pragma unroll
-      for (int j=0;j<8;j++){
-        float4 pr = *(const float4*)&params[pg*8+j][0];
-        float a0=(A0[j]-pr.x)*pr.y, a1=(A1[j]-pr.x)*pr.y;
-        float c0f=(B0[j]-pr.z)*pr.w, c1f=(B1[j]-pr.z)*pr.w;
-        *(u32*)&N2L[(pg*8+j)*144 + ch0]      = packbf2(fmaf(a0,wi0,bi0), fmaf(a1,wi1,bi1));
-        *(u32*)&N2L[(pg*8+j)*144 + 72 + ch0] = packbf2(fmaf(c0f,we0,be0), fmaf(c1f,we1,be1));
-      }
-    }
-    __syncthreads();
-    if (use_par && it < 3){
-      const int pn = p0 + 64;
-      ld8_issue(imgb, imgf, base_i + pn + pg*8, f32, rA0);
-      ld8_issue(imgb, imgf, base_i + HW + pn + pg*8, f32, rA1);
-      ld8_issue(evtb, evtf, base_i + pn + pg*8, f32, rB0);
-      ld8_issue(evtb, evtf, base_i + HW + pn + pg*8, f32, rB1);
-      const float4* pp = (const float4*)(par + ((size_t)b*HW + pn + pg*8)*4);
-      #pragma unroll
-      for (int j=0;j<8;j++) PR[j] = pp[j];
-    }
-    float4v acc1[4];
-    #pragma unroll
-    for (int nj=0;nj<4;nj++) acc1[nj]=(float4v)0.f;
-    const int px_row = wave*16 + l15;
-    #pragma unroll
-    for (int ks=0;ks<2;ks++){
-      const int off = ks*32 + quad*8;
-      short8 ai = *(const short8*)&N2L[px_row*144 + off];
-      short8 ae = *(const short8*)&N2L[px_row*144 + 72 + off];
-      #pragma unroll
-      for (int nj=0;nj<4;nj++){
-        short8 bwi = *(const short8*)&PiL[(nj*16+l15)*72 + off];
-        acc1[nj] = __builtin_amdgcn_mfma_f32_16x16x32_bf16(ai, bwi, acc1[nj], 0,0,0);
-        short8 bwe = *(const short8*)&PeL[(nj*16+l15)*72 + off];
-        acc1[nj] = __builtin_amdgcn_mfma_f32_16x16x32_bf16(ae, bwe, acc1[nj], 0,0,0);
-      }
-    }
-    float s[4], sq[4];
-    #pragma unroll
-    for (int j=0;j<4;j++){
-      s[j] = acc1[0][j]+acc1[1][j]+acc1[2][j]+acc1[3][j];
-      sq[j] = acc1[0][j]*acc1[0][j];
-      sq[j] = fmaf(acc1[1][j],acc1[1][j],sq[j]);
-      sq[j] = fmaf(acc1[2][j],acc1[2][j],sq[j]);
-      sq[j] = fmaf(acc1[3][j],acc1[3][j],sq[j]);
-    }
-    #pragma unroll
-    for (int m=1;m<=8;m<<=1)
-      #pragma unroll
-      for (int j=0;j<4;j++){ s[j]+=__shfl_xor(s[j],m); sq[j]+=__shfl_xor(sq[j],m); }
-    float muj[4], rj[4];
-    #pragma unroll
-    for (int j=0;j<4;j++){
-      muj[j]=s[j]*0.015625f;
-      rj[j]=rsqrtf(fmaf(sq[j],0.015625f,-muj[j]*muj[j])+1e-5f);
-    }
-    #pragma unroll
-    for (int nj=0;nj<4;nj++)
-      #pragma unroll
-      for (int j=0;j<4;j++){
-        float tv = (acc1[nj][j]-muj[j])*rj[j];
-        tv = fmaf(tv, w1r[nj], b1r[nj]);
-        N2L[(wave*16+quad*4+j)*144 + nj*16+l15] = f2bf(tv);
-      }
-    float4v accF[8];
-    #pragma unroll
-    for (int nh=0;nh<8;nh++) accF[nh]=(float4v)0.f;
-    #pragma unroll
-    for (int ks=0;ks<2;ks++){
-      const int off = ks*32+quad*8;
-      short8 af = *(const short8*)&N2L[px_row*144 + off];
-      #pragma unroll
-      for (int nh=0;nh<8;nh++){
-        short8 bw = *(const short8*)&fc1L[(nh*16+l15)*72 + off];
-        accF[nh] = __builtin_amdgcn_mfma_f32_16x16x32_bf16(af, bw, accF[nh], 0,0,0);
-      }
-    }
-    #pragma unroll
-    for (int nh=0;nh<8;nh++){
-      float bb = b1L[nh*16+l15];
-      #pragma unroll
-      for (int j=0;j<4;j++){
-        float v = accF[nh][j] + bb;
-        float g = 0.5f*v*(1.0f + erff(v*0.70710678118654752f));
-        N2L[(wave*16+quad*4+j)*144 + nh*16+l15] = f2bf(g);
-      }
-    }
-    float4v accO[4];
-    #pragma unroll
-    for (int nj=0;nj<4;nj++) accO[nj]=(float4v)0.f;
-    #pragma unroll
-    for (int ks=0;ks<4;ks++){
-      const int off = ks*32+quad*8;
-      short8 ag = *(const short8*)&N2L[px_row*144 + off];
-      #pragma unroll
-      for (int nj=0;nj<4;nj++){
-        short8 bw = *(const short8*)&fc2L[(nj*16+l15)*136 + off];
-        accO[nj] = __builtin_amdgcn_mfma_f32_16x16x32_bf16(ag, bw, accO[nj], 0,0,0);
-      }
-    }
-    const int px0 = p0 + wave*16 + quad*4;
-    #pragma unroll
-    for (int nj=0;nj<4;nj++){
-      float bb = b2L[nj*16+l15];
-      int r = nj*16+l15;
-      float v0 = acc1[nj][0] + accO[nj][0] + bb;
-      float v1 = acc1[nj][1] + accO[nj][1] + bb;
-      float v2 = acc1[nj][2] + accO[nj][2] + bb;
-      float v3 = acc1[nj][3] + accO[nj][3] + bb;
-      size_t oi = obase + (size_t)(b*64 + r)*HW + px0;
-      if (f32){ float4 fv; fv.x=v0; fv.y=v1; fv.z=v2; fv.w=v3;
-        *(float4*)((float*)outp + oi) = fv; }
-      else *(uint2*)((u16*)outp + oi) = make_uint2(packbf2(v0,v1), packbf2(v2,v3));
-    }
-    __syncthreads();
-  }
-}
-
 extern "C" void kernel_launch(void* const* d_in, const int* in_sizes, int n_in,
                               void* d_out, int out_size, void* d_ws, size_t ws_size,
                               hipStream_t stream)
@@ -941,24 +755,22 @@
   const int use_par = (ws_size >= WS_NEED) ? 1 : 0;
   #define SLOT(i) (wc + (size_t)((i)-2)*8192)
 
-  hipMemsetAsync(ws, 0, 131072*sizeof(float), stream);
-  convert_all<<<dim3(30), dim3(256), 0, stream>>>(img,
+  convert_all<<<dim3(32), dim3(256), 0, stream>>>(img,
       d_in[2], d_in[3], d_in[4], d_in[5], d_in[6], d_in[7], d_in[8], d_in[9],
       d_in[10], d_in[11], d_in[12], d_in[13], d_in[14], d_in[15], d_in[16], d_in[17],
       d_in[18], d_in[19], d_in[20], d_in[21], d_in[22], d_in[23], d_in[24], d_in[25],
-      d_in[26], d_in[27], d_in[28], d_in[29], d_in[30], d_in[31], wc);
+      d_in[26], d_in[27], d_in[28], d_in[29], d_in[30], d_in[31], wc, ws);
   k1_cov<<<dim3(512), dim3(512), 0, stream>>>(img, evt,
       SLOT(10), SLOT(11), SLOT(12), SLOT(13), SLOT(14), SLOT(15), SLOT(16), SLOT(17),
       ws, par, use_par);
-  p2a<<<dim3(40), dim3(256), 0, stream>>>(SLOT(2), SLOT(3), SLOT(6), SLOT(7), ws);
-  p2b<<<dim3(4), dim3(256), 0, stream>>>(ws, SLOT(2), SLOT(3), SLOT(6), SLOT(7),
-      SLOT(4), SLOT(8), SLOT(5), SLOT(9));
-  p2c<<<dim3(12), dim3(256), 0, stream>>>(SLOT(30), SLOT(31), ws);
-  k3_common<<<dim3(1024), dim3(256), 0, stream>>>(img, evt,
-      SLOT(10), SLOT(11), SLOT(12), SLOT(13), SLOT(18), SLOT(19),
-      SLOT(22), SLOT(23), SLOT(24), SLOT(25), ws + OFF_P, d_out, (size_t)0, par, use_par);
-  k3_diff<<<dim3(1024), dim3(256), 0, stream>>>(img, evt,
-      SLOT(10), SLOT(11), SLOT(12), SLOT(13), SLOT(20), SLOT(21),
-      SLOT(26), SLOT(27), SLOT(28), SLOT(29), ws + OFF_P, d_out, (size_t)16777216, par, use_par);
+  p2_fused<<<dim3(4), dim3(256), 0, stream>>>(
+      SLOT(2), SLOT(3), SLOT(6), SLOT(7), SLOT(4), SLOT(8), SLOT(5), SLOT(9),
+      SLOT(30), SLOT(31), ws);
+  k3_fat<<<dim3(2048), dim3(256), 0, stream>>>(img, evt,
+      SLOT(10), SLOT(11), SLOT(12), SLOT(13),
+      SLOT(18), SLOT(19), SLOT(20), SLOT(21),
+      SLOT(22), SLOT(23), SLOT(24), SLOT(25),
+      SLOT(26), SLOT(27), SLOT(28), SLOT(29),
+      ws + OFF_P, d_out, par, use_par);
   #undef SLOT
 }
```
